# Kernel optimization log

Measured on AMD Instinct MI355X. Metric: run time of the kernel, lower is better.

Reference implementation:

```python
import jax, jax.numpy as jnp
import numpy as np
from jax import lax

B, N, D, FD = 1, 6, 128, 128
H = W = 64
FH, FW = 32, 96
QW1, QW2 = 8, 8
KW1, KW2 = 4, 12
HEADS, DH = 4, 32
IMG_H, IMG_W = 256, 768
BN_S = 0.9999950000374996  # eval-mode BatchNorm, default stats: 1/sqrt(1+1e-5)
LN_EPS = 1e-5


def _ln(x):
    mu = x.mean(-1, keepdims=True)
    var = ((x - mu) ** 2).mean(-1, keepdims=True)
    return (x - mu) * lax.rsqrt(var + LN_EPS)


def _gelu(x):
    return jax.nn.gelu(x, approximate=False)


def _win(t, w1, w2):
    # 'b n d (x w1) (y w2) -> b n x y w1 w2 d'
    b, n, d, h, w = t.shape
    t = t.reshape(b, n, d, h // w1, w1, w // w2, w2)
    return t.transpose(0, 1, 3, 5, 4, 6, 2)


def _gridwin(t, w1, w2):
    b, n, h, w, d = t.shape
    t = t.reshape(b, n, w1, h // w1, w2, w // w2, d)
    return t.transpose(0, 1, 3, 5, 2, 4, 6)


def _cross_attend(q, k, v, qw, qb, kw, kb, vw, vb, pw, pb, skip):
    b, n, X, Y, w1, w2, d = q.shape
    k1, k2 = k.shape[4], k.shape[5]
    L, Q, K = X * Y, n * w1 * w2, n * k1 * k2
    qf = q.transpose(0, 2, 3, 1, 4, 5, 6).reshape(b, L, Q, d)
    kf = k.transpose(0, 2, 3, 1, 4, 5, 6).reshape(b, L, K, d)
    vf = v.transpose(0, 2, 3, 1, 4, 5, 6).reshape(b, L, K, d)
    qh = (_ln(qf) @ qw.T + qb).reshape(b, L, Q, HEADS, DH)
    kh = (_ln(kf) @ kw.T + kb).reshape(b, L, K, HEADS, DH)
    vh = (_ln(vf) @ vw.T + vb).reshape(b, L, K, HEADS, DH)
    dot = jnp.einsum('blqmd,blkmd->bmlqk', qh, kh) * (DH ** -0.5)
    att = jax.nn.softmax(dot, axis=-1)
    a = jnp.einsum('bmlqk,blkmd->blqmd', att, vh).reshape(b, L, Q, HEADS * DH)
    z = (a @ pw.T + pb).reshape(b, X, Y, n, w1, w2, d).mean(3)
    return z + skip


def reference(index, x, feature, I_inv, E_inv, bev_grid, fl_w, fp_w, be_w, be_b, ie_w, ce_w,
              a1_qw, a1_qb, a1_kw, a1_kb, a1_vw, a1_vb, a1_pw, a1_pb,
              a2_qw, a2_qb, a2_kw, a2_kb, a2_vw, a2_vb, a2_pw, a2_pb,
              m1_w1, m1_b1, m1_w2, m1_b2, m2_w1, m2_b1, m2_w2, m2_b2,
              mb_ew, mb_dw, mb_s1w, mb_s1b, mb_s2w, mb_s2b, mb_pw,
              pm_w1, pm_b1, pm_w2, pm_b2, po_w, po_b):
    # image-plane rays -> camera-frame directions
    xs = jnp.linspace(0.0, 1.0, FW) * IMG_W
    ys = jnp.linspace(0.0, 1.0, FH) * IMG_H
    gx, gy = jnp.meshgrid(xs, ys)                       # [FH,FW]
    pixel = jnp.stack([gx, gy, jnp.ones_like(gx)], 0).reshape(3, FH * FW)
    cam = jnp.einsum('bnij,jp->bnip', I_inv, pixel)     # [B,N,3,P]
    cam = jnp.concatenate([cam, jnp.ones_like(cam[:, :, :1])], axis=2)
    dvec = jnp.einsum('bnij,bnjp->bnip', E_inv, cam).reshape(B, N, 4, FH, FW)
    d_embed = jnp.einsum('bnchw,dc->bndhw', dvec, ie_w)            # img_embed 1x1 conv
    c_embed = jnp.einsum('bnc,dc->bnd', E_inv[..., 3], ce_w)[:, :, :, None, None]
    img_emb = d_embed - c_embed
    img_emb = img_emb / (jnp.linalg.norm(img_emb, axis=2, keepdims=True) + 1e-7)

    # BEV positional embedding (bev_embedding_flag[index] True)
    w_embed = jnp.einsum('chw,dc->dhw', bev_grid[:2], be_w) + be_b[:, None, None]
    bev_emb = w_embed[None, None] - c_embed                        # [B,N,D,H,W]
    bev_emb = bev_emb / (jnp.linalg.norm(bev_emb, axis=2, keepdims=True) + 1e-7)
    query = bev_emb + x[:, None]

    # key/value (BatchNorm eval -> ReLU -> 1x1 conv)
    f = jax.nn.relu(feature * BN_S)
    key = img_emb + jnp.einsum('bnchw,dc->bndhw', f, fp_w)
    val = jnp.einsum('bnchw,dc->bndhw', f, fl_w)

    # local-to-local windowed cross attention
    skip1 = _win(x[:, None], QW1, QW2)[:, 0]
    out1 = _cross_attend(_win(query, QW1, QW2), _win(key, KW1, KW2), _win(val, KW1, KW2),
                         a1_qw, a1_qb, a1_kw, a1_kb, a1_vw, a1_vb, a1_pw, a1_pb, skip1)
    q_img = out1.transpose(0, 1, 3, 2, 4, 5).reshape(B, H, W, D)   # 'b x y w1 w2 d -> b (x w1)(y w2) d'
    q_img = q_img + (_gelu(_ln(q_img) @ m1_w1.T + m1_b1) @ m1_w2.T + m1_b2)

    # local-to-global (grid-shuffled windows)
    x_skip = q_img
    q2 = jnp.broadcast_to(q_img[:, None], (B, N, H, W, D))
    key_hwd = key.transpose(0, 1, 3, 4, 2)
    val_hwd = val.transpose(0, 1, 3, 4, 2)
    skip2 = _gridwin(x_skip[:, None], QW1, QW2)[:, 0]
    out2 = _cross_attend(_gridwin(q2, QW1, QW2), _gridwin(key_hwd, KW1, KW2), _gridwin(val_hwd, KW1, KW2),
                         a2_qw, a2_qb, a2_kw, a2_kb, a2_vw, a2_vb, a2_pw, a2_pb, skip2)
    q_img = out2.transpose(0, 3, 1, 4, 2, 5).reshape(B, H, W, D)
    q_img = q_img + (_gelu(_ln(q_img) @ m2_w1.T + m2_b1) @ m2_w2.T + m2_b2)

    z = _ln(q_img)                                   # postnorm
    zc = z.transpose(0, 3, 1, 2)                     # [B,D,H,W]
    # MBConv (expand -> depthwise -> SE -> project, eval-mode BN, residual)
    out = _gelu(jnp.einsum('bchw,dc->bdhw', zc, mb_ew) * BN_S)
    out = lax.conv_general_dilated(out, mb_dw, (1, 1), 'SAME',
                                   dimension_numbers=('NCHW', 'OIHW', 'NCHW'),
                                   feature_group_count=out.shape[1])
    out = _gelu(out * BN_S)
    se = out.mean((2, 3), keepdims=True)
    se = _gelu(jnp.einsum('bchw,dc->bdhw', se, mb_s1w) + mb_s1b[None, :, None, None])
    se = jax.nn.sigmoid(jnp.einsum('bchw,dc->bdhw', se, mb_s2w) + mb_s2b[None, :, None, None])
    out = jnp.einsum('bchw,dc->bdhw', out * se, mb_pw) * BN_S + zc
    z = out.transpose(0, 2, 3, 1)                    # [B,H,W,D]
    z = z + (_gelu(z @ pm_w1.T + pm_b1) @ pm_w2.T + pm_b2)   # ChannelFFN
    z = _gelu(z @ po_w.T + po_b)                     # proj_out
    return z.transpose(0, 3, 1, 2)                   # [B,D,H,W]


def setup_inputs():
    ks = iter(jax.random.split(jax.random.key(0), 80))

    def rn(*s):
        return jax.random.normal(next(ks), s, dtype=jnp.float32) * 0.02

    def zz(*s):
        return jnp.zeros(s, dtype=jnp.float32)

    inp = {
        'index': 0,
        'x': jax.random.normal(next(ks), (B, D, H, W), dtype=jnp.float32),
        'feature': jax.random.normal(next(ks), (B, N, FD, FH, FW), dtype=jnp.float32),
        'I_inv': jax.random.normal(next(ks), (B, N, 3, 3), dtype=jnp.float32),
        'E_inv': jax.random.normal(next(ks), (B, N, 4, 4), dtype=jnp.float32),
        'bev_grid': jax.random.uniform(next(ks), (3, H, W), dtype=jnp.float32),
        'fl_w': rn(D, FD), 'fp_w': rn(D, FD),
        'be_w': rn(D, 2), 'be_b': zz(D), 'ie_w': rn(D, 4), 'ce_w': rn(D, 4),
    }
    for p in ('a1', 'a2'):
        for nm in ('q', 'k', 'v'):
            inp[p + '_' + nm + 'w'] = rn(HEADS * DH, D)
            inp[p + '_' + nm + 'b'] = zz(HEADS * DH)
        inp[p + '_pw'] = rn(D, HEADS * DH)
        inp[p + '_pb'] = zz(D)
    for p in ('m1', 'm2'):
        inp[p + '_w1'] = rn(2 * D, D)
        inp[p + '_b1'] = zz(2 * D)
        inp[p + '_w2'] = rn(D, 2 * D)
        inp[p + '_b2'] = zz(D)
    inp.update(mb_ew=rn(4 * D, D), mb_dw=rn(4 * D, 1, 3, 3),
               mb_s1w=rn(32, 4 * D), mb_s1b=zz(32), mb_s2w=rn(4 * D, 32), mb_s2b=zz(4 * D),
               mb_pw=rn(D, 4 * D),
               pm_w1=rn(2 * D, D), pm_b1=zz(2 * D), pm_w2=rn(D, 2 * D), pm_b2=zz(D),
               po_w=rn(D, D), po_b=zz(D))
    return inp
```

## Files before the change

kernel.cpp:

```cpp
#include <hip/hip_runtime.h>
#include <math.h>

#define NV 6
#define FHH 32
#define FWW 96
#define PIMG (FHH*FWW)
#define HH 64
#define WWD 64
#define PBEV (HH*WWD)
#define HEADS 4
#define DHD 32
#define KROWS 288
#define BN_S 0.9999950000374996f
#define LN_EPS 1e-5f
#define ATT_SCALE 0.17677669529663687f

typedef __attribute__((ext_vector_type(8))) short short8;
typedef __attribute__((ext_vector_type(4))) float f32x4;
typedef __attribute__((ext_vector_type(8))) unsigned short u16x8;

__device__ __forceinline__ float gelu_f(float x) {
    return 0.5f * x * (1.0f + erff(x * 0.70710678118654752f));
}

__device__ __forceinline__ unsigned short f2bf(float f) {
    union { float f; unsigned int u; } c; c.f = f;
    unsigned int r = (c.u + 0x7fffu + ((c.u >> 16) & 1u)) >> 16;
    return (unsigned short)r;
}

__device__ __forceinline__ float bf2f(unsigned short u) {
    union { unsigned int u; float f; } c; c.u = ((unsigned int)u) << 16;
    return c.f;
}

#define OFF_FP    0
#define OFF_FL    16384
#define OFF_A1QW  32768
#define OFF_A1KW  49152
#define OFF_A2KW  65536
#define OFF_A1VW  81920
#define OFF_A2VW  98304
#define OFF_A1PW  114688
#define OFF_M1W1  131072
#define OFF_M1W2  163840
#define OFF_A2QW  196608
#define OFF_A2PW  212992
#define OFF_M2W1  229376
#define OFF_M2W2  262144
#define OFF_MBEW  294912
#define OFF_MBPW  360448
#define OFF_PMW1  425984
#define OFF_PMW2  458752
#define OFF_POW   491520
#define WTOTAL    507904

__global__ void k_cvtw(const float* p0, const float* p1, const float* p2,
                       const float* p3, const float* p4, const float* p5,
                       const float* p6, const float* p7, const float* p8,
                       const float* p9, const float* p10, const float* p11,
                       const float* p12, const float* p13, const float* p14,
                       const float* p15, const float* p16, const float* p17,
                       const float* p18, unsigned short* wb) {
    int idx = (blockIdx.x * 256 + threadIdx.x) * 8;
    if (idx >= WTOTAL) return;
    const float* s;
    if      (idx < OFF_FL)   s = p0  + idx;
    else if (idx < OFF_A1QW) s = p1  + (idx - OFF_FL);
    else if (idx < OFF_A1KW) s = p2  + (idx - OFF_A1QW);
    else if (idx < OFF_A2KW) s = p3  + (idx - OFF_A1KW);
    else if (idx < OFF_A1VW) s = p4  + (idx - OFF_A2KW);
    else if (idx < OFF_A2VW) s = p5  + (idx - OFF_A1VW);
    else if (idx < OFF_A1PW) s = p6  + (idx - OFF_A2VW);
    else if (idx < OFF_M1W1) s = p7  + (idx - OFF_A1PW);
    else if (idx < OFF_M1W2) s = p8  + (idx - OFF_M1W1);
    else if (idx < OFF_A2QW) s = p9  + (idx - OFF_M1W2);
    else if (idx < OFF_A2PW) s = p10 + (idx - OFF_A2QW);
    else if (idx < OFF_M2W1) s = p11 + (idx - OFF_A2PW);
    else if (idx < OFF_M2W2) s = p12 + (idx - OFF_M2W1);
    else if (idx < OFF_MBEW) s = p13 + (idx - OFF_M2W2);
    else if (idx < OFF_MBPW) s = p14 + (idx - OFF_MBEW);
    else if (idx < OFF_PMW1) s = p15 + (idx - OFF_MBPW);
    else if (idx < OFF_PMW2) s = p16 + (idx - OFF_PMW1);
    else if (idx < OFF_POW)  s = p17 + (idx - OFF_PMW2);
    else                     s = p18 + (idx - OFF_POW);
    float4 v0 = *(const float4*)&s[0];
    float4 v1 = *(const float4*)&s[4];
    u16x8 o = { f2bf(v0.x), f2bf(v0.y), f2bf(v0.z), f2bf(v0.w),
                f2bf(v1.x), f2bf(v1.y), f2bf(v1.z), f2bf(v1.w) };
    *(u16x8*)&wb[idx] = o;
}

__global__ void k_transx(const float* __restrict__ x, float* __restrict__ x_cl) {
    __shared__ float tile[32][33];
    int c0 = blockIdx.y * 32, p0 = blockIdx.x * 32;
    int tp = threadIdx.x & 31, tg = threadIdx.x >> 5;
    #pragma unroll
    for (int i = 0; i < 4; ++i)
        tile[tg + 8 * i][tp] = x[(size_t)(c0 + tg + 8 * i) * PBEV + p0 + tp];
    __syncthreads();
    #pragma unroll
    for (int i = 0; i < 4; ++i)
        x_cl[(size_t)(p0 + tg + 8 * i) * 128 + c0 + tp] = tile[tp][tg + 8 * i];
}

template<int BR, int KCH, int NOT, int AMODE, int LNF, int BIASF, int ACT, int SCL,
         int ADDM, int STM, int ASCL, int DUAL, int OUTBF, int QSCL, int WRLN,
         int EMB, int WBF>
__global__ __launch_bounds__(256)
void k_gemm_mfma(const float* __restrict__ A, const float* __restrict__ W,
                 const float* __restrict__ bias, const float* __restrict__ addb,
                 const float* __restrict__ ascale, const float* __restrict__ W2,
                 const float* __restrict__ bias2, void* __restrict__ out2v,
                 float* __restrict__ aux, void* __restrict__ outv) {
    constexpr int NI = KCH * 128;
    constexpr int RW = BR / 16;
    constexpr int CT = 8 / (4 / RW);
    __shared__ unsigned short Al[BR * 136];
    __shared__ unsigned short Wl[128 * 136];
    const int t = threadIdx.x;
    const int rb = blockIdx.x * BR;
    const int co = blockIdx.y * 128;
    const int lane = t & 63, wv = t >> 6;
    const int la = lane & 15, g = lane >> 4;
    const int roww = wv % RW, colg = wv / RW;

    if constexpr (KCH == 1) {
        if constexpr (AMODE == 1) {
            int n = rb / PIMG, p0 = rb % PIMG;
            int r = t & 63, kseg = t >> 6;
            #pragma unroll
            for (int j8 = 0; j8 < 4; ++j8) {
                u16x8 o;
                #pragma unroll
                for (int j = 0; j < 8; ++j) {
                    int k = kseg * 32 + j8 * 8 + j;
                    float v = A[((size_t)(n * 128 + k)) * PIMG + p0 + r];
                    o[j] = f2bf(fmaxf(v * BN_S, 0.0f));
                }
                *(u16x8*)&Al[r * 136 + kseg * 32 + j8 * 8] = o;
            }
        } else {
            constexpr int TPR = 256 / BR;
            constexpr int CPT = 128 / TPR;
            int r = t / TPR, seg = t % TPR;
            float v[CPT];
            if constexpr (AMODE == 3) {
                int grow = rb + r;
                int n = grow >> 12, p = grow & 4095;
                const float* E = ((const float*)out2v) + n * 16;
                const float* cew = (const float*)aux;
                float bp0 = addb[p], bp1 = addb[PBEV + p];
                float ss = 0.f;
                #pragma unroll
                for (int j = 0; j < CPT; ++j) {
                    int c = seg * CPT + j;
                    float cemb = E[3]  * cew[c*4+0] + E[7]  * cew[c*4+1]
                               + E[11] * cew[c*4+2] + E[15] * cew[c*4+3];
                    float emb = bp0 * W2[c*2] + bp1 * W2[c*2+1] + bias2[c] - cemb;
                    v[j] = emb; ss += emb * emb;
                }
                #pragma unroll
                for (int o = 1; o < TPR; o <<= 1) ss += __shfl_xor(ss, o, 64);
                float invn = 1.0f / (sqrtf(ss) + 1e-7f);
                const float* xr = ascale + (size_t)p * 128 + seg * CPT;
                #pragma unroll
                for (int j = 0; j < CPT; ++j) v[j] = v[j] * invn + xr[j];
            } else if constexpr (AMODE == 4) {
                const unsigned short* ab = ((const unsigned short*)A)
                    + (size_t)(rb + r) * 128 + seg * CPT;
                #pragma unroll
                for (int j8 = 0; j8 < CPT / 8; ++j8) {
                    u16x8 raw = *(const u16x8*)&ab[8 * j8];
                    #pragma unroll
                    for (int j = 0; j < 8; ++j) v[8 * j8 + j] = bf2f(raw[j]);
                }
            } else {
                const float* ar = A + (size_t)(rb + r) * 128 + seg * CPT;
                #pragma unroll
                for (int j4 = 0; j4 < CPT / 4; ++j4)
                    *(float4*)&v[4 * j4] = *(const float4*)&ar[4 * j4];
            }
            if constexpr (LNF) {
                float s = 0.f;
                #pragma unroll
                for (int j = 0; j < CPT; ++j) s += v[j];
                #pragma unroll
                for (int o = 1; o < TPR; o <<= 1) s += __shfl_xor(s, o, 64);
                float mu = s * (1.0f / 128.0f);
                float ss = 0.f;
                #pragma unroll
                for (int j = 0; j < CPT; ++j) { float d = v[j] - mu; ss += d * d; }
                #pragma unroll
                for (int o = 1; o < TPR; o <<= 1) ss += __shfl_xor(ss, o, 64);
                float rs = rsqrtf(ss * (1.0f / 128.0f) + LN_EPS);
                #pragma unroll
                for (int j = 0; j < CPT; ++j) v[j] = (v[j] - mu) * rs;
                if constexpr (WRLN) {
                    if (blockIdx.y == 0) {
                        #pragma unroll
                        for (int j4 = 0; j4 < CPT / 4; ++j4) {
                            float4 o4 = {v[4*j4], v[4*j4+1], v[4*j4+2], v[4*j4+3]};
                            *(float4*)&aux[(size_t)(rb + r) * 128 + seg * CPT + 4 * j4] = o4;
                        }
                    }
                }
            }
            #pragma unroll
            for (int j8 = 0; j8 < CPT / 8; ++j8) {
                u16x8 o;
                #pragma unroll
                for (int j = 0; j < 8; ++j) o[j] = f2bf(v[8 * j8 + j]);
                *(u16x8*)&Al[r * 136 + seg * CPT + 8 * j8] = o;
            }
        }
    }

    #pragma unroll 1
    for (int set = 0; set <= DUAL; ++set) {
        const float* Wc = set ? W2 : W;
        const float* bc = set ? bias2 : bias;
        void* ocv = set ? out2v : outv;
        f32x4 acc[CT];
        #pragma unroll
        for (int i = 0; i < CT; ++i) acc[i] = (f32x4){0.f, 0.f, 0.f, 0.f};

        #pragma unroll 1
        for (int kc = 0; kc < KCH; ++kc) {
            if (set || kc) __syncthreads();
            #pragma unroll
            for (int i = 0; i < 8; ++i) {
                int chunk = i * 256 + t;
                int c = chunk >> 4, k8 = chunk & 15;
                if constexpr (WBF) {
                    const unsigned short* wr = ((const unsigned short*)Wc)
                        + (size_t)(co + c) * NI + kc * 128 + k8 * 8;
                    *(u16x8*)&Wl[c * 136 + k8 * 8] = *(const u16x8*)wr;
                } else {
                    const float* wr = &Wc[(size_t)(co + c) * NI + kc * 128 + k8 * 8];
                    float4 v0 = *(const float4*)&wr[0];
                    float4 v1 = *(const float4*)&wr[4];
                    u16x8 o = { f2bf(v0.x), f2bf(v0.y), f2bf(v0.z), f2bf(v0.w),
                                f2bf(v1.x), f2bf(v1.y), f2bf(v1.z), f2bf(v1.w) };
                    *(u16x8*)&Wl[c * 136 + k8 * 8] = o;
                }
            }
            __syncthreads();
            short8 af[4];
            #pragma unroll
            for (int ks = 0; ks < 4; ++ks)
                af[ks] = *(short8*)&Al[(roww * 16 + la) * 136 + ks * 32 + g * 8];
            #pragma unroll
            for (int cti = 0; cti < CT; ++cti) {
                int ct = colg * CT + cti;
                #pragma unroll
                for (int ks = 0; ks < 4; ++ks) {
                    short8 bf = *(short8*)&Wl[(ct * 16 + la) * 136 + ks * 32 + g * 8];
                    acc[cti] = __builtin_amdgcn_mfma_f32_16x16x32_bf16(af[ks], bf, acc[cti], 0, 0, 0);
                }
            }
        }

        float embv[CT][4];
        float invr[4];
        if constexpr (EMB) {
            if (set == 0) {
                int n = rb / PIMG;
                const float* Ii = ascale + n * 9;
                const float* E  = addb + n * 16;
                float d0[4], d1[4], d2[4], d3[4];
                #pragma unroll
                for (int r = 0; r < 4; ++r) {
                    int row = rb + roww * 16 + g * 4 + r;
                    int p = row % PIMG;
                    int hh = p / FWW, wp = p % FWW;
                    float gx = (float)wp * (768.0f / 95.0f);
                    float gy = (float)hh * (256.0f / 31.0f);
                    float c0 = Ii[0]*gx + Ii[1]*gy + Ii[2];
                    float c1 = Ii[3]*gx + Ii[4]*gy + Ii[5];
                    float c2 = Ii[6]*gx + Ii[7]*gy + Ii[8];
                    d0[r] = E[0]*c0  + E[1]*c1  + E[2]*c2  + E[3];
                    d1[r] = E[4]*c0  + E[5]*c1  + E[6]*c2  + E[7];
                    d2[r] = E[8]*c0  + E[9]*c1  + E[10]*c2 + E[11];
                    d3[r] = E[12]*c0 + E[13]*c1 + E[14]*c2 + E[15];
                }
                float ssr[4] = {0.f, 0.f, 0.f, 0.f};
                #pragma unroll
                for (int cti = 0; cti < CT; ++cti) {
                    int col = co + (colg * CT + cti) * 16 + la;
                    const float* iw = bias + col * 4;
                    const float* cw = bias2 + col * 4;
                    float cemb = E[3]*cw[0] + E[7]*cw[1] + E[11]*cw[2] + E[15]*cw[3];
                    #pragma unroll
                    for (int r = 0; r < 4; ++r) {
                        float e = d0[r]*iw[0] + d1[r]*iw[1] + d2[r]*iw[2] + d3[r]*iw[3] - cemb;
                        embv[cti][r] = e;
                        ssr[r] += e * e;
                    }
                }
                #pragma unroll
                for (int r = 0; r < 4; ++r) {
                    float s = ssr[r];
                    s += __shfl_xor(s, 1); s += __shfl_xor(s, 2);
                    s += __shfl_xor(s, 4); s += __shfl_xor(s, 8);
                    invr[r] = 1.0f / (sqrtf(s) + 1e-7f);
                }
            }
        }

        #pragma unroll
        for (int cti = 0; cti < CT; ++cti) {
            int ct = colg * CT + cti;
            int col = co + ct * 16 + la;
            float bv = 0.f;
            if constexpr (BIASF) bv = bc[col];
            if constexpr (STM == 1) {
                int row0 = rb + roww * 16 + g * 4;
                float vv[4];
                #pragma unroll
                for (int r = 0; r < 4; ++r) {
                    float v = acc[cti][r] + bv;
                    if constexpr (SCL)  v *= BN_S;
                    if constexpr (ACT)  v = gelu_f(v);
                    if constexpr (QSCL) v *= ATT_SCALE;
                    vv[r] = v;
                }
                float4 o4 = {vv[0], vv[1], vv[2], vv[3]};
                *(float4*)&((float*)ocv)[(size_t)col * PBEV + row0] = o4;
            } else {
                #pragma unroll
                for (int r = 0; r < 4; ++r) {
                    int row = rb + roww * 16 + g * 4 + r;
                    float v = acc[cti][r] + bv;
                    if constexpr (SCL)  v *= BN_S;
                    if constexpr (ACT)  v = gelu_f(v);
                    if constexpr (QSCL) v *= ATT_SCALE;
                    if constexpr (EMB) { if (set == 0) v += embv[cti][r] * invr[r]; }
                    if constexpr (ADDM == 1) { if (set == 0) v += addb[(size_t)row * 128 + col]; }
                    if constexpr (ADDM == 2) { if (set == 0) v += addb[(size_t)col * PBEV + row]; }
                    if constexpr (OUTBF) ((unsigned short*)ocv)[(size_t)row * NOT + col] = f2bf(v);
                    else                 ((float*)ocv)[(size_t)row * NOT + col] = v;
                }
            }
        }
    }
}

struct KVJob {
    const unsigned short* A;
    const unsigned short* W1;
    const float* b1;
    const unsigned short* W2;
    const float* b2;
    unsigned short* o1;
    unsigned short* o2;
};

__global__ __launch_bounds__(256)
void k_kvheads(KVJob jk, KVJob jv) {
    const KVJob j = (blockIdx.x < 288) ? jk : jv;
    const int rb = (blockIdx.x % 288) * 64;
    __shared__ unsigned short Al[64 * 136];
    __shared__ unsigned short Wl[128 * 136];
    const int t = threadIdx.x;
    const int lane = t & 63, wv = t >> 6;
    const int la = lane & 15, g = lane >> 4;

    {
        int r = t >> 2, seg = t & 3;
        const unsigned short* ab = j.A + (size_t)(rb + r) * 128 + seg * 32;
        float v[32];
        #pragma unroll
        for (int j8 = 0; j8 < 4; ++j8) {
            u16x8 raw = *(const u16x8*)&ab[8 * j8];
            #pragma unroll
            for (int jj = 0; jj < 8; ++jj) v[8 * j8 + jj] = bf2f(raw[jj]);
        }
        float s = 0.f;
        #pragma unroll
        for (int jj = 0; jj < 32; ++jj) s += v[jj];
        s += __shfl_xor(s, 1); s += __shfl_xor(s, 2);
        float mu = s * (1.0f / 128.0f);
        float ss = 0.f;
        #pragma unroll
        for (int jj = 0; jj < 32; ++jj) { float d = v[jj] - mu; ss += d * d; }
        ss += __shfl_xor(ss, 1); ss += __shfl_xor(ss, 2);
        float rs = rsqrtf(ss * (1.0f / 128.0f) + LN_EPS);
        #pragma unroll
        for (int j8 = 0; j8 < 4; ++j8) {
            u16x8 o;
            #pragma unroll
            for (int jj = 0; jj < 8; ++jj) o[jj] = f2bf((v[8 * j8 + jj] - mu) * rs);
            *(u16x8*)&Al[r * 136 + seg * 32 + 8 * j8] = o;
        }
    }

    #pragma unroll 1
    for (int set = 0; set < 2; ++set) {
        const unsigned short* Wc = set ? j.W2 : j.W1;
        const float* bc = set ? j.b2 : j.b1;
        unsigned short* oc = set ? j.o2 : j.o1;
        if (set) __syncthreads();
        #pragma unroll
        for (int i = 0; i < 8; ++i) {
            int chunk = i * 256 + t;
            int c = chunk >> 4, k8 = chunk & 15;
            *(u16x8*)&Wl[c * 136 + k8 * 8] =
                *(const u16x8*)&Wc[(size_t)c * 128 + k8 * 8];
        }
        __syncthreads();
        short8 af[4];
        #pragma unroll
        for (int ks = 0; ks < 4; ++ks)
            af[ks] = *(short8*)&Al[(wv * 16 + la) * 136 + ks * 32 + g * 8];
        #pragma unroll
        for (int ct = 0; ct < 8; ++ct) {
            f32x4 acc = (f32x4){0.f, 0.f, 0.f, 0.f};
            #pragma unroll
            for (int ks = 0; ks < 4; ++ks) {
                short8 bf = *(short8*)&Wl[(ct * 16 + la) * 136 + ks * 32 + g * 8];
                acc = __builtin_amdgcn_mfma_f32_16x16x32_bf16(af[ks], bf, acc, 0, 0, 0);
            }
            int col = ct * 16 + la;
            float bv = bc[col];
            #pragma unroll
            for (int r = 0; r < 4; ++r) {
                int row = rb + wv * 16 + g * 4 + r;
                oc[(size_t)row * 128 + col] = f2bf(acc[r] + bv);
            }
        }
    }
}

template<int AM>
__global__ __launch_bounds__(256)
void k_projmlp(const float* __restrict__ Ain, const unsigned short* __restrict__ pwb,
               const float* __restrict__ pb, const float* __restrict__ resid,
               const unsigned short* __restrict__ w1b, const float* __restrict__ b1,
               const unsigned short* __restrict__ w2b, const float* __restrict__ b2,
               float* __restrict__ out) {
    __shared__ unsigned short Al[16 * 136];
    __shared__ unsigned short Wl[128 * 72];
    __shared__ unsigned short Gl[16 * 264];
    __shared__ float Xf[16 * 132];
    const int t = threadIdx.x;
    const int rb = blockIdx.x * 16;
    const int lane = t & 63, wv = t >> 6;
    const int la = lane & 15, g = lane >> 4;

    {
        int r = t >> 4, seg = t & 15;
        float v[8];
        if constexpr (AM == 2) {
            int hw = rb + r;
            int h = hw >> 6, w = hw & 63;
            int l = (h >> 3) * 8 + (w >> 3), ww = (h & 7) * 8 + (w & 7);
            const float* src = Ain + ((size_t)(l * 64 + ww)) * 6 * 128 + seg * 8;
            #pragma unroll
            for (int jj = 0; jj < 8; ++jj) v[jj] = 0.f;
            #pragma unroll
            for (int n = 0; n < 6; ++n) {
                float4 x0 = *(const float4*)&src[n * 128];
                float4 x1 = *(const float4*)&src[n * 128 + 4];
                v[0] += x0.x; v[1] += x0.y; v[2] += x0.z; v[3] += x0.w;
                v[4] += x1.x; v[5] += x1.y; v[6] += x1.z; v[7] += x1.w;
            }
            #pragma unroll
            for (int jj = 0; jj < 8; ++jj) v[jj] *= (1.0f / 6.0f);
        } else {
            const float* ar = Ain + (size_t)(rb + r) * 128 + seg * 8;
            *(float4*)&v[0] = *(const float4*)&ar[0];
            *(float4*)&v[4] = *(const float4*)&ar[4];
        }
        u16x8 o;
        #pragma unroll
        for (int jj = 0; jj < 8; ++jj) o[jj] = f2bf(v[jj]);
        *(u16x8*)&Al[r * 136 + seg * 8] = o;
    }
    __syncthreads();

    f32x4 acc2[2];
    acc2[0] = (f32x4){0.f, 0.f, 0.f, 0.f};
    acc2[1] = (f32x4){0.f, 0.f, 0.f, 0.f};
    #pragma unroll 1
    for (int kc = 0; kc < 2; ++kc) {
        if (kc) __syncthreads();
        {
            int c = t >> 1, s2 = t & 1;
            const unsigned short* wr = pwb + (size_t)c * 128 + kc * 64 + s2 * 32;
            #pragma unroll
            for (int j8 = 0; j8 < 4; ++j8)
                *(u16x8*)&Wl[c * 72 + s2 * 32 + 8 * j8] = *(const u16x8*)&wr[8 * j8];
        }
        __syncthreads();
        #pragma unroll
        for (int half = 0; half < 2; ++half) {
            short8 pf = *(short8*)&Al[la * 136 + kc * 64 + half * 32 + g * 8];
            #pragma unroll
            for (int ct = 0; ct < 2; ++ct) {
                short8 bf = *(short8*)&Wl[((wv * 2 + ct) * 16 + la) * 72 + half * 32 + g * 8];
                acc2[ct] = __builtin_amdgcn_mfma_f32_16x16x32_bf16(pf, bf, acc2[ct], 0, 0, 0);
            }
        }
    }
    __syncthreads();
    #pragma unroll
    for (int ct = 0; ct < 2; ++ct) {
        int col = (wv * 2 + ct) * 16 + la;
        float bv = pb[col];
        #pragma unroll
        for (int r = 0; r < 4; ++r) {
            int row = g * 4 + r;
            Xf[row * 132 + col] = acc2[ct][r] + bv
                                + resid[(size_t)(rb + row) * 128 + col];
        }
    }
    __syncthreads();

    {
        int r = t >> 4, seg = t & 15;
        float v[8];
        #pragma unroll
        for (int jj = 0; jj < 8; ++jj) v[jj] = Xf[r * 132 + seg * 8 + jj];
        float s = 0.f;
        #pragma unroll
        for (int jj = 0; jj < 8; ++jj) s += v[jj];
        s += __shfl_xor(s, 1); s += __shfl_xor(s, 2);
        s += __shfl_xor(s, 4); s += __shfl_xor(s, 8);
        float mu = s * (1.0f / 128.0f);
        float ss = 0.f;
        #pragma unroll
        for (int jj = 0; jj < 8; ++jj) { float d = v[jj] - mu; ss += d * d; }
        ss += __shfl_xor(ss, 1); ss += __shfl_xor(ss, 2);
        ss += __shfl_xor(ss, 4); ss += __shfl_xor(ss, 8);
        float rs = rsqrtf(ss * (1.0f / 128.0f) + LN_EPS);
        u16x8 o;
        #pragma unroll
        for (int jj = 0; jj < 8; ++jj) o[jj] = f2bf((v[jj] - mu) * rs);
        *(u16x8*)&Al[r * 136 + seg * 8] = o;
    }
    __syncthreads();

    short8 af[4];
    #pragma unroll
    for (int ks = 0; ks < 4; ++ks)
        af[ks] = *(short8*)&Al[la * 136 + ks * 32 + g * 8];

    #pragma unroll 1
    for (int cc = 0; cc < 4; ++cc) {
        {
            int c = t >> 2, s2 = t & 3;
            const unsigned short* wr = w1b + (size_t)(cc * 64 + c) * 128 + s2 * 32;
            #pragma unroll
            for (int j8 = 0; j8 < 4; ++j8)
                *(u16x8*)&Wl[c * 136 + s2 * 32 + 8 * j8] = *(const u16x8*)&wr[8 * j8];
        }
        __syncthreads();
        f32x4 acc = (f32x4){0.f, 0.f, 0.f, 0.f};
        #pragma unroll
        for (int ks = 0; ks < 4; ++ks) {
            short8 bf = *(short8*)&Wl[(wv * 16 + la) * 136 + ks * 32 + g * 8];
            acc = __builtin_amdgcn_mfma_f32_16x16x32_bf16(af[ks], bf, acc, 0, 0, 0);
        }
        int col = cc * 64 + wv * 16 + la;
        float bv = b1[col];
        #pragma unroll
        for (int r = 0; r < 4; ++r)
            Gl[(g * 4 + r) * 264 + col] = f2bf(gelu_f(acc[r] + bv));
        __syncthreads();
    }

    acc2[0] = (f32x4){0.f, 0.f, 0.f, 0.f};
    acc2[1] = (f32x4){0.f, 0.f, 0.f, 0.f};
    #pragma unroll 1
    for (int kc = 0; kc < 4; ++kc) {
        {
            int c = t >> 1, s2 = t & 1;
            const unsigned short* wr = w2b + (size_t)c * 256 + kc * 64 + s2 * 32;
            #pragma unroll
            for (int j8 = 0; j8 < 4; ++j8)
                *(u16x8*)&Wl[c * 72 + s2 * 32 + 8 * j8] = *(const u16x8*)&wr[8 * j8];
        }
        __syncthreads();
        #pragma unroll
        for (int half = 0; half < 2; ++half) {
            short8 pf = *(short8*)&Gl[la * 264 + kc * 64 + half * 32 + g * 8];
            #pragma unroll
            for (int ct = 0; ct < 2; ++ct) {
                short8 bf = *(short8*)&Wl[((wv * 2 + ct) * 16 + la) * 72 + half * 32 + g * 8];
                acc2[ct] = __builtin_amdgcn_mfma_f32_16x16x32_bf16(pf, bf, acc2[ct], 0, 0, 0);
            }
        }
        __syncthreads();
    }
    #pragma unroll
    for (int ct = 0; ct < 2; ++ct) {
        int col = (wv * 2 + ct) * 16 + la;
        float bv = b2[col];
        #pragma unroll
        for (int r = 0; r < 4; ++r) {
            int row = g * 4 + r;
            out[(size_t)(rb + row) * 128 + col] = acc2[ct][r] + bv + Xf[row * 132 + col];
        }
    }
}

__global__ __launch_bounds__(256)
void k_mbprojmlp(const float* __restrict__ dwo, const unsigned short* __restrict__ mbpwb,
                 const float* __restrict__ se, const float* __restrict__ zln,
                 const unsigned short* __restrict__ w1b, const float* __restrict__ b1,
                 const unsigned short* __restrict__ w2b, const float* __restrict__ b2,
                 const unsigned short* __restrict__ pob, const float* __restrict__ pb,
                 float* __restrict__ out) {
    __shared__ unsigned short Al[16 * 136];
    __shared__ unsigned short Wl[128 * 72];
    __shared__ unsigned short Gl[16 * 264];
    __shared__ float Xf[16 * 132];
    const int t = threadIdx.x;
    const int rb = blockIdx.x * 16;
    const int lane = t & 63, wv = t >> 6;
    const int la = lane & 15, g = lane >> 4;

    f32x4 acc2[2];
    acc2[0] = (f32x4){0.f, 0.f, 0.f, 0.f};
    acc2[1] = (f32x4){0.f, 0.f, 0.f, 0.f};
    #pragma unroll 1
    for (int kc = 0; kc < 8; ++kc) {
        if (kc) __syncthreads();
        {
            int r = t >> 4, seg = t & 15;
            const float* ar = dwo + (size_t)(rb + r) * 512 + kc * 64 + seg * 4;
            float4 v = *(const float4*)ar;
            const float* sp = se + kc * 64 + seg * 4;
            v.x *= sp[0]; v.y *= sp[1]; v.z *= sp[2]; v.w *= sp[3];
            unsigned short* dst = &Al[r * 136 + seg * 4];
            dst[0] = f2bf(v.x); dst[1] = f2bf(v.y);
            dst[2] = f2bf(v.z); dst[3] = f2bf(v.w);
        }
        {
            int c = t >> 1, s2 = t & 1;
            const unsigned short* wr = mbpwb + (size_t)c * 512 + kc * 64 + s2 * 32;
            #pragma unroll
            for (int j8 = 0; j8 < 4; ++j8)
                *(u16x8*)&Wl[c * 72 + s2 * 32 + 8 * j8] = *(const u16x8*)&wr[8 * j8];
        }
        __syncthreads();
        #pragma unroll
        for (int half = 0; half < 2; ++half) {
            short8 pf = *(short8*)&Al[la * 136 + half * 32 + g * 8];
            #pragma unroll
            for (int ct = 0; ct < 2; ++ct) {
                short8 bf = *(short8*)&Wl[((wv * 2 + ct) * 16 + la) * 72 + half * 32 + g * 8];
                acc2[ct] = __builtin_amdgcn_mfma_f32_16x16x32_bf16(pf, bf, acc2[ct], 0, 0, 0);
            }
        }
    }
    __syncthreads();
    #pragma unroll
    for (int ct = 0; ct < 2; ++ct) {
        int col = (wv * 2 + ct) * 16 + la;
        #pragma unroll
        for (int r = 0; r < 4; ++r) {
            int row = g * 4 + r;
            Xf[row * 132 + col] = acc2[ct][r] * BN_S
                                + zln[(size_t)(rb + row) * 128 + col];
        }
    }
    __syncthreads();

    {
        int r = t >> 4, seg = t & 15;
        u16x8 o;
        #pragma unroll
        for (int jj = 0; jj < 8; ++jj) o[jj] = f2bf(Xf[r * 132 + seg * 8 + jj]);
        *(u16x8*)&Al[r * 136 + seg * 8] = o;
    }
    __syncthreads();

    short8 af[4];
    #pragma unroll
    for (int ks = 0; ks < 4; ++ks)
        af[ks] = *(short8*)&Al[la * 136 + ks * 32 + g * 8];

    #pragma unroll 1
    for (int cc = 0; cc < 4; ++cc) {
        {
            int c = t >> 2, s2 = t & 3;
            const unsigned short* wr = w1b + (size_t)(cc * 64 + c) * 128 + s2 * 32;
            #pragma unroll
            for (int j8 = 0; j8 < 4; ++j8)
                *(u16x8*)&Wl[c * 136 + s2 * 32 + 8 * j8] = *(const u16x8*)&wr[8 * j8];
        }
        __syncthreads();
        f32x4 acc = (f32x4){0.f, 0.f, 0.f, 0.f};
        #pragma unroll
        for (int ks = 0; ks < 4; ++ks) {
            short8 bf = *(short8*)&Wl[(wv * 16 + la) * 136 + ks * 32 + g * 8];
            acc = __builtin_amdgcn_mfma_f32_16x16x32_bf16(af[ks], bf, acc, 0, 0, 0);
        }
        int col = cc * 64 + wv * 16 + la;
        float bv = b1[col];
        #pragma unroll
        for (int r = 0; r < 4; ++r)
            Gl[(g * 4 + r) * 264 + col] = f2bf(gelu_f(acc[r] + bv));
        __syncthreads();
    }

    acc2[0] = (f32x4){0.f, 0.f, 0.f, 0.f};
    acc2[1] = (f32x4){0.f, 0.f, 0.f, 0.f};
    #pragma unroll 1
    for (int kc = 0; kc < 4; ++kc) {
        {
            int c = t >> 1, s2 = t & 1;
            const unsigned short* wr = w2b + (size_t)c * 256 + kc * 64 + s2 * 32;
            #pragma unroll
            for (int j8 = 0; j8 < 4; ++j8)
                *(u16x8*)&Wl[c * 72 + s2 * 32 + 8 * j8] = *(const u16x8*)&wr[8 * j8];
        }
        __syncthreads();
        #pragma unroll
        for (int half = 0; half < 2; ++half) {
            short8 pf = *(short8*)&Gl[la * 264 + kc * 64 + half * 32 + g * 8];
            #pragma unroll
            for (int ct = 0; ct < 2; ++ct) {
                short8 bf = *(short8*)&Wl[((wv * 2 + ct) * 16 + la) * 72 + half * 32 + g * 8];
                acc2[ct] = __builtin_amdgcn_mfma_f32_16x16x32_bf16(pf, bf, acc2[ct], 0, 0, 0);
            }
        }
        __syncthreads();
    }
    #pragma unroll
    for (int ct = 0; ct < 2; ++ct) {
        int col = (wv * 2 + ct) * 16 + la;
        float bv = b2[col];
        #pragma unroll
        for (int r = 0; r < 4; ++r) {
            int row = g * 4 + r;
            float y = acc2[ct][r] + bv + Xf[row * 132 + col];
            Al[row * 136 + col] = f2bf(y);
        }
    }
    __syncthreads();

    f32x4 acc3[2];
    acc3[0] = (f32x4){0.f, 0.f, 0.f, 0.f};
    acc3[1] = (f32x4){0.f, 0.f, 0.f, 0.f};
    #pragma unroll 1
    for (int kc = 0; kc < 2; ++kc) {
        if (kc) __syncthreads();
        {
            int c = t >> 1, s2 = t & 1;
            const unsigned short* wr = pob + (size_t)c * 128 + kc * 64 + s2 * 32;
            #pragma unroll
            for (int j8 = 0; j8 < 4; ++j8)
                *(u16x8*)&Wl[c * 72 + s2 * 32 + 8 * j8] = *(const u16x8*)&wr[8 * j8];
        }
        __syncthreads();
        #pragma unroll
        for (int half = 0; half < 2; ++half) {
            short8 pf = *(short8*)&Al[la * 136 + kc * 64 + half * 32 + g * 8];
            #pragma unroll
            for (int ct = 0; ct < 2; ++ct) {
                short8 bf = *(short8*)&Wl[((wv * 2 + ct) * 16 + la) * 72 + half * 32 + g * 8];
                acc3[ct] = __builtin_amdgcn_mfma_f32_16x16x32_bf16(pf, bf, acc3[ct], 0, 0, 0);
            }
        }
    }
    #pragma unroll
    for (int ct = 0; ct < 2; ++ct) {
        int col = (wv * 2 + ct) * 16 + la;
        float bv = pb[col];
        float4 o4;
        o4.x = gelu_f(acc3[ct][0] + bv);
        o4.y = gelu_f(acc3[ct][1] + bv);
        o4.z = gelu_f(acc3[ct][2] + bv);
        o4.w = gelu_f(acc3[ct][3] + bv);
        *(float4*)&out[(size_t)col * PBEV + rb + g * 4] = o4;
    }
}

template<int MODE>
__global__ __launch_bounds__(MODE == 1 ? 512 : 256)
void k_attn_mfma(const unsigned short* __restrict__ qh, const unsigned short* __restrict__ kh,
                 const unsigned short* __restrict__ vh, float* __restrict__ aout) {
    constexpr int WAVES = (MODE == 1) ? 8 : 4;
    constexpr int QTPW  = (MODE == 1) ? 3 : 1;
    constexpr int T = WAVES * 64;
    const int l = blockIdx.x, m = blockIdx.y;
    const int xw = l >> 3, yw = l & 7;
    const int t = threadIdx.x;
    const int lane = t & 63, wv = t >> 6;
    const int la = lane & 15, g = lane >> 4;

    __shared__ unsigned short Kl[KROWS * 40];
    __shared__ unsigned short Vt[32 * 312];

    for (int i = t; i < KROWS * 4; i += T) {
        int row = i >> 2, seg = i & 3;
        int n = row / 48, kk = row % 48;
        int k1 = kk / 12, k2 = kk % 12;
        int h, w;
        if (MODE == 1) { h = xw * 4 + k1;  w = yw * 12 + k2; }
        else           { h = k1 * 8 + xw;  w = k2 * 8 + yw;  }
        size_t src = ((size_t)(n * PIMG + h * FWW + w)) * 128 + m * DHD + seg * 8;
        short8 kv = *(const short8*)&kh[src];
        *(short8*)&Kl[row * 40 + seg * 8] = kv;
        short8 vv = *(const short8*)&vh[src];
        #pragma unroll
        for (int j = 0; j < 8; ++j)
            Vt[(seg * 8 + j) * 312 + row] = (unsigned short)vv[j];
    }

    short8 qf[QTPW];
    #pragma unroll
    for (int qt = 0; qt < QTPW; ++qt) {
        int q = (wv * QTPW + qt) * 16 + la;
        int row;
        if (MODE == 1) {
            int n = q >> 6, ww = q & 63;
            row = n * PBEV + (xw * 8 + (ww >> 3)) * 64 + yw * 8 + (ww & 7);
        } else {
            row = ((q >> 3) * 8 + xw) * 64 + (q & 7) * 8 + yw;
        }
        qf[qt] = *(const short8*)&qh[(size_t)row * 128 + m * DHD + g * 8];
    }
    __syncthreads();

    f32x4 acc[QTPW][2];
    float srow[QTPW];
    #pragma unroll
    for (int qt = 0; qt < QTPW; ++qt) {
        acc[qt][0] = (f32x4){0.f, 0.f, 0.f, 0.f};
        acc[qt][1] = (f32x4){0.f, 0.f, 0.f, 0.f};
        srow[qt] = 0.f;
    }
    const int a0 = la + 32 * (g & 1);
    const int a1 = a0 + 16;
    const bool selA = (g < 2);

    #pragma unroll 1
    for (int c = 0; c < 9; ++c) {
        const int kk0 = c * 32;
        short8 kf0 = *(short8*)&Kl[(kk0 + la) * 40 + g * 8];
        short8 kf1 = *(short8*)&Kl[(kk0 + 16 + la) * 40 + g * 8];
        short8 vf0 = *(short8*)&Vt[la * 312 + kk0 + g * 8];
        short8 vf1 = *(short8*)&Vt[(16 + la) * 312 + kk0 + g * 8];
        #pragma unroll
        for (int qt = 0; qt < QTPW; ++qt) {
            f32x4 sA = __builtin_amdgcn_mfma_f32_16x16x32_bf16(kf0, qf[qt], (f32x4){0.f,0.f,0.f,0.f}, 0, 0, 0);
            f32x4 sB = __builtin_amdgcn_mfma_f32_16x16x32_bf16(kf1, qf[qt], (f32x4){0.f,0.f,0.f,0.f}, 0, 0, 0);
            float pA[4], pB[4];
            #pragma unroll
            for (int r = 0; r < 4; ++r) { pA[r] = __expf(sA[r]); pB[r] = __expf(sB[r]); }
            srow[qt] += ((pA[0] + pA[1]) + (pA[2] + pA[3]))
                      + ((pB[0] + pB[1]) + (pB[2] + pB[3]));
            unsigned int loA = (unsigned int)f2bf(pA[0]) | ((unsigned int)f2bf(pA[1]) << 16);
            unsigned int hiA = (unsigned int)f2bf(pA[2]) | ((unsigned int)f2bf(pA[3]) << 16);
            unsigned int loB = (unsigned int)f2bf(pB[0]) | ((unsigned int)f2bf(pB[1]) << 16);
            unsigned int hiB = (unsigned int)f2bf(pB[2]) | ((unsigned int)f2bf(pB[3]) << 16);
            int w0A = __shfl((int)loA, a0); int w0B = __shfl((int)loB, a0);
            int w1A = __shfl((int)hiA, a0); int w1B = __shfl((int)hiB, a0);
            int w2A = __shfl((int)loA, a1); int w2B = __shfl((int)loB, a1);
            int w3A = __shfl((int)hiA, a1); int w3B = __shfl((int)hiB, a1);
            union { int u[4]; short8 s; } pu;
            pu.u[0] = selA ? w0A : w0B;
            pu.u[1] = selA ? w1A : w1B;
            pu.u[2] = selA ? w2A : w2B;
            pu.u[3] = selA ? w3A : w3B;
            acc[qt][0] = __builtin_amdgcn_mfma_f32_16x16x32_bf16(pu.s, vf0, acc[qt][0], 0, 0, 0);
            acc[qt][1] = __builtin_amdgcn_mfma_f32_16x16x32_bf16(pu.s, vf1, acc[qt][1], 0, 0, 0);
        }
    }

    #pragma unroll
    for (int qt = 0; qt < QTPW; ++qt) {
        float s = srow[qt];
        s += __shfl_xor(s, 16);
        s += __shfl_xor(s, 32);
        #pragma unroll
        for (int r = 0; r < 4; ++r) {
            float sq = __shfl(s, g * 4 + r);
            float inv = 1.0f / sq;
            int q = (wv * QTPW + qt) * 16 + g * 4 + r;
            size_t orow;
            if (MODE == 1) {
                int n = q >> 6, ww = q & 63;
                orow = (size_t)(l * 64 + ww) * 6 + n;
            } else {
                orow = (size_t)(((q >> 3) * 8 + xw) * 64 + (q & 7) * 8 + yw);
            }
            float* ap = aout + orow * 128 + m * DHD;
            ap[la]      = acc[qt][0][r] * inv;
            ap[16 + la] = acc[qt][1][r] * inv;
        }
    }
}

__global__ void k_dwconv(const float* __restrict__ ex, const float* __restrict__ dwgt,
                         float* __restrict__ dwout, float* __restrict__ separt) {
    const int TILE = 16;
    int ch = threadIdx.x;
    int hw0 = blockIdx.x * TILE;
    float wreg[9];
    #pragma unroll
    for (int i = 0; i < 9; ++i) wreg[i] = dwgt[ch * 9 + i];
    float sacc = 0.f;
    for (int ti = 0; ti < TILE; ++ti) {
        int hw = hw0 + ti;
        int h = hw >> 6, w = hw & 63;
        float s = 0.f;
        #pragma unroll
        for (int dy = -1; dy <= 1; ++dy) {
            int h2 = h + dy;
            if (h2 < 0 || h2 >= 64) continue;
            #pragma unroll
            for (int dx = -1; dx <= 1; ++dx) {
                int w2 = w + dx;
                if (w2 < 0 || w2 >= 64) continue;
                s += ex[((size_t)(h2 * 64 + w2)) * 512 + ch] * wreg[(dy + 1) * 3 + (dx + 1)];
            }
        }
        float o = gelu_f(s * BN_S);
        dwout[(size_t)hw * 512 + ch] = o;
        sacc += o;
    }
    separt[(size_t)blockIdx.x * 512 + ch] = sacc;
}

__global__ void k_sered(const float* __restrict__ separt, float* __restrict__ separt2) {
    int t = threadIdx.x, bb = blockIdx.x;
    float s = 0.f;
    #pragma unroll
    for (int i = 0; i < 16; ++i)
        s += separt[(size_t)(bb * 16 + i) * 512 + t];
    separt2[(size_t)bb * 512 + t] = s;
}

__global__ void k_se(const float* __restrict__ separt2,
                     const float* __restrict__ s1w, const float* __restrict__ s1b,
                     const float* __restrict__ s2w, const float* __restrict__ s2b,
                     float* __restrict__ se) {
    __shared__ float mean[512];
    __shared__ float s1[32];
    int t = threadIdx.x;
    float s = 0.f;
    #pragma unroll
    for (int b = 0; b < 16; ++b) s += separt2[b * 512 + t];
    mean[t] = s * (1.0f / 4096.0f);
    __syncthreads();
    int u = t >> 4, seg = t & 15;
    float acc = 0.f;
    #pragma unroll
    for (int j = 0; j < 32; ++j) {
        int c = seg + 16 * j;
        acc += mean[c] * s1w[u * 512 + c];
    }
    acc += __shfl_xor(acc, 1); acc += __shfl_xor(acc, 2);
    acc += __shfl_xor(acc, 4); acc += __shfl_xor(acc, 8);
    if (seg == 0) s1[u] = gelu_f(acc + s1b[u]);
    __syncthreads();
    float a2 = s2b[t];
    #pragma unroll
    for (int j = 0; j < 32; ++j) a2 += s1[j] * s2w[t * 32 + j];
    se[t] = 1.0f / (1.0f + __expf(-a2));
}

extern "C" void kernel_launch(void* const* d_in, const int* in_sizes, int n_in,
                              void* d_out, int out_size, void* d_ws, size_t ws_size,
                              hipStream_t stream) {
    (void)in_sizes; (void)n_in; (void)out_size; (void)ws_size;
    const float* x      = (const float*)d_in[1];
    const float* feat   = (const float*)d_in[2];
    const float* I_inv  = (const float*)d_in[3];
    const float* E_inv  = (const float*)d_in[4];
    const float* bev    = (const float*)d_in[5];
    const float* fl_w   = (const float*)d_in[6];
    const float* fp_w   = (const float*)d_in[7];
    const float* be_w   = (const float*)d_in[8];
    const float* be_b   = (const float*)d_in[9];
    const float* ie_w   = (const float*)d_in[10];
    const float* ce_w   = (const float*)d_in[11];
    const float* a1_qw  = (const float*)d_in[12];
    const float* a1_qb  = (const float*)d_in[13];
    const float* a1_kw  = (const float*)d_in[14];
    const float* a1_kb  = (const float*)d_in[15];
    const float* a1_vw  = (const float*)d_in[16];
    const float* a1_vb  = (const float*)d_in[17];
    const float* a1_pw  = (const float*)d_in[18];
    const float* a1_pb  = (const float*)d_in[19];
    const float* a2_qw  = (const float*)d_in[20];
    const float* a2_qb  = (const float*)d_in[21];
    const float* a2_kw  = (const float*)d_in[22];
    const float* a2_kb  = (const float*)d_in[23];
    const float* a2_vw  = (const float*)d_in[24];
    const float* a2_vb  = (const float*)d_in[25];
    const float* a2_pw  = (const float*)d_in[26];
    const float* a2_pb  = (const float*)d_in[27];
    const float* m1_w1  = (const float*)d_in[28];
    const float* m1_b1  = (const float*)d_in[29];
    const float* m1_w2  = (const float*)d_in[30];
    const float* m1_b2  = (const float*)d_in[31];
    const float* m2_w1  = (const float*)d_in[32];
    const float* m2_b1  = (const float*)d_in[33];
    const float* m2_w2  = (const float*)d_in[34];
    const float* m2_b2  = (const float*)d_in[35];
    const float* mb_ew  = (const float*)d_in[36];
    const float* mb_dw  = (const float*)d_in[37];
    const float* mb_s1w = (const float*)d_in[38];
    const float* mb_s1b = (const float*)d_in[39];
    const float* mb_s2w = (const float*)d_in[40];
    const float* mb_s2b = (const float*)d_in[41];
    const float* mb_pw  = (const float*)d_in[42];
    const float* pm_w1  = (const float*)d_in[43];
    const float* pm_b1  = (const float*)d_in[44];
    const float* pm_w2  = (const float*)d_in[45];
    const float* pm_b2  = (const float*)d_in[46];
    const float* po_w   = (const float*)d_in[47];
    const float* po_b   = (const float*)d_in[48];

    float* ws = (float*)d_ws;
    float* x_cl   = ws + 0;
    unsigned short* key_b = (unsigned short*)(ws + 524288);
    unsigned short* val_b = (unsigned short*)(ws + 1703936);
    unsigned short* qh1b  = (unsigned short*)(ws + 2883584);
    unsigned short* kh1b  = (unsigned short*)(ws + 4456448);
    unsigned short* vh1b  = (unsigned short*)(ws + 5636096);
    unsigned short* kh2b  = (unsigned short*)(ws + 6815744);
    unsigned short* vh2b  = (unsigned short*)(ws + 7995392);
    float* abuf   = ws + 9175040;
    float* qimg   = ws + 12320768;
    float* qimg2  = ws + 12845056;
    float* zln    = ws + 13369344;
    float* abuf2  = ws + 13893632;
    float* expandb = ws + 14942208;
    float* dwout   = ws + 17039360;
    float* separt  = ws + 19136512;
    float* separt2 = ws + 19267584;
    float* sebuf   = ws + 19275776;
    unsigned short* wb = (unsigned short*)(ws + 19276288);
    unsigned short* qh2b = qh1b;

    k_cvtw<<<248, 256, 0, stream>>>(fp_w, fl_w, a1_qw, a1_kw, a2_kw, a1_vw, a2_vw,
                                    a1_pw, m1_w1, m1_w2, a2_qw, a2_pw, m2_w1, m2_w2,
                                    mb_ew, mb_pw, pm_w1, pm_w2, po_w, wb);
    k_transx<<<dim3(128, 4), 256, 0, stream>>>(x, x_cl);

    k_gemm_mfma<64,1,128, 1,0,0,0,0, 0,0,0,1, 1,0,0,1,1><<<288, 256, 0, stream>>>(
        feat, (const float*)(wb + OFF_FP), ie_w, E_inv, I_inv,
        (const float*)(wb + OFF_FL), ce_w, val_b, nullptr, key_b);

    k_gemm_mfma<64,1,128, 3,1,1,0,0, 0,0,0,0, 1,1,0,0,1><<<384, 256, 0, stream>>>(
        nullptr, (const float*)(wb + OFF_A1QW), a1_qb, bev, x_cl, be_w, be_b,
        (void*)E_inv, (float*)ce_w, qh1b);
    {
        KVJob jk = { key_b, wb + OFF_A1KW, a1_kb, wb + OFF_A2KW, a2_kb, kh1b, kh2b };
        KVJob jv = { val_b, wb + OFF_A1VW, a1_vb, wb + OFF_A2VW, a2_vb, vh1b, vh2b };
        k_kvheads<<<576, 256, 0, stream>>>(jk, jv);
    }
    k_attn_mfma<1><<<dim3(64, HEADS), 512, 0, stream>>>(qh1b, kh1b, vh1b, abuf);
    k_projmlp<2><<<256, 256, 0, stream>>>(abuf, wb + OFF_A1PW, a1_pb, x_cl,
                                          wb + OFF_M1W1, m1_b1, wb + OFF_M1W2, m1_b2, qimg);

    k_gemm_mfma<16,1,128, 0,1,1,0,0, 0,0,0,0, 1,1,0,0,1><<<256, 256, 0, stream>>>(
        qimg, (const float*)(wb + OFF_A2QW), a2_qb, nullptr, nullptr, nullptr,
        nullptr, nullptr, nullptr, qh2b);
    k_attn_mfma<2><<<dim3(64, HEADS), 256, 0, stream>>>(qh2b, kh2b, vh2b, abuf2);
    k_projmlp<0><<<256, 256, 0, stream>>>(abuf2, wb + OFF_A2PW, a2_pb, qimg,
                                          wb + OFF_M2W1, m2_b1, wb + OFF_M2W2, m2_b2, qimg2);

    k_gemm_mfma<16,1,512, 0,1,0,1,1, 0,0,0,0, 0,0,1,0,1><<<dim3(256, 4), 256, 0, stream>>>(
        qimg2, (const float*)(wb + OFF_MBEW), nullptr, nullptr, nullptr, nullptr,
        nullptr, nullptr, zln, expandb);
    k_dwconv<<<256, 512, 0, stream>>>(expandb, mb_dw, dwout, separt);
    k_sered<<<16, 512, 0, stream>>>(separt, separt2);
    k_se<<<1, 512, 0, stream>>>(separt2, mb_s1w, mb_s1b, mb_s2w, mb_s2b, sebuf);
    k_mbprojmlp<<<256, 256, 0, stream>>>(dwout, wb + OFF_MBPW, sebuf, zln,
                                         wb + OFF_PMW1, pm_b1, wb + OFF_PMW2, pm_b2,
                                         wb + OFF_POW, po_b, (float*)d_out);
}
```

Before: 155.2 us.

## Fuse key/value feature and head projections, merge prep kernels, average views in attention

Weight conversion and the BEV transpose are merged into one launch. The feature-to-key/value GEMMs, camera embedding, LayerNorm and all four per-head K/V projections now run in a single kernel that keeps intermediates in shared memory, so the key_b/val_b round trip through global memory goes away. The first attention reduces the per-view mean in shared memory with atomics and writes an averaged buffer, which lets the projection-MLP skip that averaging. The SE partial-sum kernel is folded into the SE kernel. Together these cut launches and memory traffic, at the cost of serial per-block work and shared-memory atomics.

```diff
diff --git a/kernel.cpp b/kernel.cpp
--- a/kernel.cpp
+++ b/kernel.cpp
@@ -27,11 +27,6 @@
     union { float f; unsigned int u; } c; c.f = f;
     unsigned int r = (c.u + 0x7fffu + ((c.u >> 16) & 1u)) >> 16;
     return (unsigned short)r;
-}
-
-__device__ __forceinline__ float bf2f(unsigned short u) {
-    union { unsigned int u; float f; } c; c.u = ((unsigned int)u) << 16;
-    return c.f;
 }
 
 #define OFF_FP    0
@@ -55,65 +50,232 @@
 #define OFF_POW   491520
 #define WTOTAL    507904
 
-__global__ void k_cvtw(const float* p0, const float* p1, const float* p2,
+__global__ void k_prep(const float* p0, const float* p1, const float* p2,
                        const float* p3, const float* p4, const float* p5,
                        const float* p6, const float* p7, const float* p8,
                        const float* p9, const float* p10, const float* p11,
                        const float* p12, const float* p13, const float* p14,
                        const float* p15, const float* p16, const float* p17,
-                       const float* p18, unsigned short* wb) {
-    int idx = (blockIdx.x * 256 + threadIdx.x) * 8;
-    if (idx >= WTOTAL) return;
-    const float* s;
-    if      (idx < OFF_FL)   s = p0  + idx;
-    else if (idx < OFF_A1QW) s = p1  + (idx - OFF_FL);
-    else if (idx < OFF_A1KW) s = p2  + (idx - OFF_A1QW);
-    else if (idx < OFF_A2KW) s = p3  + (idx - OFF_A1KW);
-    else if (idx < OFF_A1VW) s = p4  + (idx - OFF_A2KW);
-    else if (idx < OFF_A2VW) s = p5  + (idx - OFF_A1VW);
-    else if (idx < OFF_A1PW) s = p6  + (idx - OFF_A2VW);
-    else if (idx < OFF_M1W1) s = p7  + (idx - OFF_A1PW);
-    else if (idx < OFF_M1W2) s = p8  + (idx - OFF_M1W1);
-    else if (idx < OFF_A2QW) s = p9  + (idx - OFF_M1W2);
-    else if (idx < OFF_A2PW) s = p10 + (idx - OFF_A2QW);
-    else if (idx < OFF_M2W1) s = p11 + (idx - OFF_A2PW);
-    else if (idx < OFF_M2W2) s = p12 + (idx - OFF_M2W1);
-    else if (idx < OFF_MBEW) s = p13 + (idx - OFF_M2W2);
-    else if (idx < OFF_MBPW) s = p14 + (idx - OFF_MBEW);
-    else if (idx < OFF_PMW1) s = p15 + (idx - OFF_MBPW);
-    else if (idx < OFF_PMW2) s = p16 + (idx - OFF_PMW1);
-    else if (idx < OFF_POW)  s = p17 + (idx - OFF_PMW2);
-    else                     s = p18 + (idx - OFF_POW);
-    float4 v0 = *(const float4*)&s[0];
-    float4 v1 = *(const float4*)&s[4];
-    u16x8 o = { f2bf(v0.x), f2bf(v0.y), f2bf(v0.z), f2bf(v0.w),
-                f2bf(v1.x), f2bf(v1.y), f2bf(v1.z), f2bf(v1.w) };
-    *(u16x8*)&wb[idx] = o;
+                       const float* p18, unsigned short* wb,
+                       const float* __restrict__ x, float* __restrict__ x_cl) {
+    __shared__ float tile[32][33];
+    if (blockIdx.x < 248) {
+        int idx = (blockIdx.x * 256 + threadIdx.x) * 8;
+        if (idx >= WTOTAL) return;
+        const float* s;
+        if      (idx < OFF_FL)   s = p0  + idx;
+        else if (idx < OFF_A1QW) s = p1  + (idx - OFF_FL);
+        else if (idx < OFF_A1KW) s = p2  + (idx - OFF_A1QW);
+        else if (idx < OFF_A2KW) s = p3  + (idx - OFF_A1KW);
+        else if (idx < OFF_A1VW) s = p4  + (idx - OFF_A2KW);
+        else if (idx < OFF_A2VW) s = p5  + (idx - OFF_A1VW);
+        else if (idx < OFF_A1PW) s = p6  + (idx - OFF_A2VW);
+        else if (idx < OFF_M1W1) s = p7  + (idx - OFF_A1PW);
+        else if (idx < OFF_M1W2) s = p8  + (idx - OFF_M1W1);
+        else if (idx < OFF_A2QW) s = p9  + (idx - OFF_M1W2);
+        else if (idx < OFF_A2PW) s = p10 + (idx - OFF_A2QW);
+        else if (idx < OFF_M2W1) s = p11 + (idx - OFF_A2PW);
+        else if (idx < OFF_M2W2) s = p12 + (idx - OFF_M2W1);
+        else if (idx < OFF_MBEW) s = p13 + (idx - OFF_M2W2);
+        else if (idx < OFF_MBPW) s = p14 + (idx - OFF_MBEW);
+        else if (idx < OFF_PMW1) s = p15 + (idx - OFF_MBPW);
+        else if (idx < OFF_PMW2) s = p16 + (idx - OFF_PMW1);
+        else if (idx < OFF_POW)  s = p17 + (idx - OFF_PMW2);
+        else                     s = p18 + (idx - OFF_POW);
+        float4 v0 = *(const float4*)&s[0];
+        float4 v1 = *(const float4*)&s[4];
+        u16x8 o = { f2bf(v0.x), f2bf(v0.y), f2bf(v0.z), f2bf(v0.w),
+                    f2bf(v1.x), f2bf(v1.y), f2bf(v1.z), f2bf(v1.w) };
+        *(u16x8*)&wb[idx] = o;
+    } else {
+        int bb = blockIdx.x - 248;
+        int p0_ = (bb & 127) * 32, c0 = (bb >> 7) * 32;
+        int tp = threadIdx.x & 31, tg = threadIdx.x >> 5;
+        #pragma unroll
+        for (int i = 0; i < 4; ++i)
+            tile[tg + 8 * i][tp] = x[(size_t)(c0 + tg + 8 * i) * PBEV + p0_ + tp];
+        __syncthreads();
+        #pragma unroll
+        for (int i = 0; i < 4; ++i)
+            x_cl[(size_t)(p0_ + tg + 8 * i) * 128 + c0 + tp] = tile[tp][tg + 8 * i];
+    }
 }
 
-__global__ void k_transx(const float* __restrict__ x, float* __restrict__ x_cl) {
-    __shared__ float tile[32][33];
-    int c0 = blockIdx.y * 32, p0 = blockIdx.x * 32;
-    int tp = threadIdx.x & 31, tg = threadIdx.x >> 5;
-    #pragma unroll
-    for (int i = 0; i < 4; ++i)
-        tile[tg + 8 * i][tp] = x[(size_t)(c0 + tg + 8 * i) * PBEV + p0 + tp];
-    __syncthreads();
-    #pragma unroll
-    for (int i = 0; i < 4; ++i)
-        x_cl[(size_t)(p0 + tg + 8 * i) * 128 + c0 + tp] = tile[tp][tg + 8 * i];
+__global__ __launch_bounds__(256)
+void k_keyval(const float* __restrict__ feat, const unsigned short* __restrict__ wb,
+              const float* __restrict__ ie_w, const float* __restrict__ ce_w,
+              const float* __restrict__ I_inv, const float* __restrict__ E_inv,
+              const float* __restrict__ a1_kb, const float* __restrict__ a2_kb,
+              const float* __restrict__ a1_vb, const float* __restrict__ a2_vb,
+              unsigned short* __restrict__ kh1b, unsigned short* __restrict__ kh2b,
+              unsigned short* __restrict__ vh1b, unsigned short* __restrict__ vh2b) {
+    __shared__ unsigned short Al[64 * 136];
+    __shared__ unsigned short Bl[64 * 136];
+    __shared__ unsigned short Wl[128 * 136];
+    const int t = threadIdx.x;
+    const int rb = blockIdx.x * 64;
+    const int n = rb / PIMG;
+    const int lane = t & 63, wv = t >> 6;
+    const int la = lane & 15, g = lane >> 4;
+
+    {
+        int p0 = rb % PIMG;
+        int r = t & 63, kseg = t >> 6;
+        #pragma unroll
+        for (int j8 = 0; j8 < 4; ++j8) {
+            u16x8 o;
+            #pragma unroll
+            for (int j = 0; j < 8; ++j) {
+                int k = kseg * 32 + j8 * 8 + j;
+                float v = feat[((size_t)(n * 128 + k)) * PIMG + p0 + r];
+                o[j] = f2bf(fmaxf(v * BN_S, 0.0f));
+            }
+            *(u16x8*)&Al[r * 136 + kseg * 32 + j8 * 8] = o;
+        }
+    }
+
+    float d0[4], d1[4], d2[4], d3[4];
+    {
+        const float* Ii = I_inv + n * 9;
+        const float* E  = E_inv + n * 16;
+        #pragma unroll
+        for (int r = 0; r < 4; ++r) {
+            int row = rb + wv * 16 + g * 4 + r;
+            int p = row % PIMG;
+            int hh = p / FWW, wp = p % FWW;
+            float gx = (float)wp * (768.0f / 95.0f);
+            float gy = (float)hh * (256.0f / 31.0f);
+            float c0 = Ii[0]*gx + Ii[1]*gy + Ii[2];
+            float c1 = Ii[3]*gx + Ii[4]*gy + Ii[5];
+            float c2 = Ii[6]*gx + Ii[7]*gy + Ii[8];
+            d0[r] = E[0]*c0  + E[1]*c1  + E[2]*c2  + E[3];
+            d1[r] = E[4]*c0  + E[5]*c1  + E[6]*c2  + E[7];
+            d2[r] = E[8]*c0  + E[9]*c1  + E[10]*c2 + E[11];
+            d3[r] = E[12]*c0 + E[13]*c1 + E[14]*c2 + E[15];
+        }
+    }
+
+    #pragma unroll 1
+    for (int kv = 0; kv < 2; ++kv) {
+        __syncthreads();
+        {
+            const unsigned short* Wf = wb + (kv ? OFF_FL : OFF_FP);
+            #pragma unroll
+            for (int i = 0; i < 8; ++i) {
+                int chunk = i * 256 + t;
+                int c = chunk >> 4, k8 = chunk & 15;
+                *(u16x8*)&Wl[c * 136 + k8 * 8] = *(const u16x8*)&Wf[(size_t)c * 128 + k8 * 8];
+            }
+        }
+        __syncthreads();
+        short8 af[4];
+        #pragma unroll
+        for (int ks = 0; ks < 4; ++ks)
+            af[ks] = *(short8*)&Al[(wv * 16 + la) * 136 + ks * 32 + g * 8];
+        float vacc[8][4];
+        #pragma unroll
+        for (int ct = 0; ct < 8; ++ct) {
+            f32x4 a = (f32x4){0.f, 0.f, 0.f, 0.f};
+            #pragma unroll
+            for (int ks = 0; ks < 4; ++ks) {
+                short8 bf = *(short8*)&Wl[(ct * 16 + la) * 136 + ks * 32 + g * 8];
+                a = __builtin_amdgcn_mfma_f32_16x16x32_bf16(af[ks], bf, a, 0, 0, 0);
+            }
+            #pragma unroll
+            for (int r = 0; r < 4; ++r) vacc[ct][r] = a[r];
+        }
+        if (kv == 0) {
+            const float* E = E_inv + n * 16;
+            float embv[8][4];
+            float ssr[4] = {0.f, 0.f, 0.f, 0.f};
+            #pragma unroll
+            for (int ct = 0; ct < 8; ++ct) {
+                int col = ct * 16 + la;
+                const float* iw = ie_w + col * 4;
+                const float* cw = ce_w + col * 4;
+                float cemb = E[3]*cw[0] + E[7]*cw[1] + E[11]*cw[2] + E[15]*cw[3];
+                #pragma unroll
+                for (int r = 0; r < 4; ++r) {
+                    float e = d0[r]*iw[0] + d1[r]*iw[1] + d2[r]*iw[2] + d3[r]*iw[3] - cemb;
+                    embv[ct][r] = e;
+                    ssr[r] += e * e;
+                }
+            }
+            #pragma unroll
+            for (int r = 0; r < 4; ++r) {
+                float s = ssr[r];
+                s += __shfl_xor(s, 1); s += __shfl_xor(s, 2);
+                s += __shfl_xor(s, 4); s += __shfl_xor(s, 8);
+                float inv = 1.0f / (sqrtf(s) + 1e-7f);
+                #pragma unroll
+                for (int ct = 0; ct < 8; ++ct) vacc[ct][r] += embv[ct][r] * inv;
+            }
+        }
+        #pragma unroll
+        for (int r = 0; r < 4; ++r) {
+            float s = 0.f;
+            #pragma unroll
+            for (int ct = 0; ct < 8; ++ct) s += vacc[ct][r];
+            s += __shfl_xor(s, 1); s += __shfl_xor(s, 2);
+            s += __shfl_xor(s, 4); s += __shfl_xor(s, 8);
+            float mu = s * (1.0f / 128.0f);
+            float ss = 0.f;
+            #pragma unroll
+            for (int ct = 0; ct < 8; ++ct) { float d = vacc[ct][r] - mu; ss += d * d; }
+            ss += __shfl_xor(ss, 1); ss += __shfl_xor(ss, 2);
+            ss += __shfl_xor(ss, 4); ss += __shfl_xor(ss, 8);
+            float rs = rsqrtf(ss * (1.0f / 128.0f) + LN_EPS);
+            int brow = wv * 16 + g * 4 + r;
+            #pragma unroll
+            for (int ct = 0; ct < 8; ++ct)
+                Bl[brow * 136 + ct * 16 + la] = f2bf((vacc[ct][r] - mu) * rs);
+        }
+
+        #pragma unroll 1
+        for (int hs = 0; hs < 2; ++hs) {
+            __syncthreads();
+            const unsigned short* Wh = wb + (kv == 0 ? (hs ? OFF_A2KW : OFF_A1KW)
+                                                     : (hs ? OFF_A2VW : OFF_A1VW));
+            const float* hb = kv == 0 ? (hs ? a2_kb : a1_kb) : (hs ? a2_vb : a1_vb);
+            unsigned short* oc = kv == 0 ? (hs ? kh2b : kh1b) : (hs ? vh2b : vh1b);
+            #pragma unroll
+            for (int i = 0; i < 8; ++i) {
+                int chunk = i * 256 + t;
+                int c = chunk >> 4, k8 = chunk & 15;
+                *(u16x8*)&Wl[c * 136 + k8 * 8] = *(const u16x8*)&Wh[(size_t)c * 128 + k8 * 8];
+            }
+            __syncthreads();
+            short8 af2[4];
+            #pragma unroll
+            for (int ks = 0; ks < 4; ++ks)
+                af2[ks] = *(short8*)&Bl[(wv * 16 + la) * 136 + ks * 32 + g * 8];
+            #pragma unroll
+            for (int ct = 0; ct < 8; ++ct) {
+                f32x4 a = (f32x4){0.f, 0.f, 0.f, 0.f};
+                #pragma unroll
+                for (int ks = 0; ks < 4; ++ks) {
+                    short8 bf = *(short8*)&Wl[(ct * 16 + la) * 136 + ks * 32 + g * 8];
+                    a = __builtin_amdgcn_mfma_f32_16x16x32_bf16(af2[ks], bf, a, 0, 0, 0);
+                }
+                int col = ct * 16 + la;
+                float bv = hb[col];
+                #pragma unroll
+                for (int r = 0; r < 4; ++r)
+                    oc[(size_t)(rb + wv * 16 + g * 4 + r) * 128 + col] = f2bf(a[r] + bv);
+            }
+        }
+    }
 }
 
-template<int BR, int KCH, int NOT, int AMODE, int LNF, int BIASF, int ACT, int SCL,
-         int ADDM, int STM, int ASCL, int DUAL, int OUTBF, int QSCL, int WRLN,
-         int EMB, int WBF>
+template<int BR, int NOT, int AMODE, int LNF, int BIASF, int ACT, int SCL,
+         int OUTBF, int QSCL, int WRLN>
 __global__ __launch_bounds__(256)
-void k_gemm_mfma(const float* __restrict__ A, const float* __restrict__ W,
-                 const float* __restrict__ bias, const float* __restrict__ addb,
-                 const float* __restrict__ ascale, const float* __restrict__ W2,
-                 const float* __restrict__ bias2, void* __restrict__ out2v,
-                 float* __restrict__ aux, void* __restrict__ outv) {
-    constexpr int NI = KCH * 128;
+void k_gemm_mfma(const float* __restrict__ A, const unsigned short* __restrict__ Wb,
+                 const float* __restrict__ bias, const float* __restrict__ bev,
+                 const float* __restrict__ x_cl, const float* __restrict__ be_w,
+                 const float* __restrict__ be_b, const float* __restrict__ E_inv,
+                 const float* __restrict__ ce_w, float* __restrict__ aux,
+                 void* __restrict__ outv) {
     constexpr int RW = BR / 16;
     constexpr int CT = 8 / (4 / RW);
     __shared__ unsigned short Al[BR * 136];
@@ -125,314 +287,108 @@
     const int la = lane & 15, g = lane >> 4;
     const int roww = wv % RW, colg = wv / RW;
 
-    if constexpr (KCH == 1) {
-        if constexpr (AMODE == 1) {
-            int n = rb / PIMG, p0 = rb % PIMG;
-            int r = t & 63, kseg = t >> 6;
-            #pragma unroll
-            for (int j8 = 0; j8 < 4; ++j8) {
-                u16x8 o;
-                #pragma unroll
-                for (int j = 0; j < 8; ++j) {
-                    int k = kseg * 32 + j8 * 8 + j;
-                    float v = A[((size_t)(n * 128 + k)) * PIMG + p0 + r];
-                    o[j] = f2bf(fmaxf(v * BN_S, 0.0f));
-                }
-                *(u16x8*)&Al[r * 136 + kseg * 32 + j8 * 8] = o;
-            }
+    {
+        constexpr int TPR = 256 / BR;
+        constexpr int CPT = 128 / TPR;
+        int r = t / TPR, seg = t % TPR;
+        float v[CPT];
+        if constexpr (AMODE == 3) {
+            int grow = rb + r;
+            int n = grow >> 12, p = grow & 4095;
+            const float* E = E_inv + n * 16;
+            float bp0 = bev[p], bp1 = bev[PBEV + p];
+            float ss = 0.f;
+            #pragma unroll
+            for (int j = 0; j < CPT; ++j) {
+                int c = seg * CPT + j;
+                float cemb = E[3]  * ce_w[c*4+0] + E[7]  * ce_w[c*4+1]
+                           + E[11] * ce_w[c*4+2] + E[15] * ce_w[c*4+3];
+                float emb = bp0 * be_w[c*2] + bp1 * be_w[c*2+1] + be_b[c] - cemb;
+                v[j] = emb; ss += emb * emb;
+            }
+            #pragma unroll
+            for (int o = 1; o < TPR; o <<= 1) ss += __shfl_xor(ss, o, 64);
+            float invn = 1.0f / (sqrtf(ss) + 1e-7f);
+            const float* xr = x_cl + (size_t)p * 128 + seg * CPT;
+            #pragma unroll
+            for (int j = 0; j < CPT; ++j) v[j] = v[j] * invn + xr[j];
         } else {
-            constexpr int TPR = 256 / BR;
-            constexpr int CPT = 128 / TPR;
-            int r = t / TPR, seg = t % TPR;
-            float v[CPT];
-            if constexpr (AMODE == 3) {
-                int grow = rb + r;
-                int n = grow >> 12, p = grow & 4095;
-                const float* E = ((const float*)out2v) + n * 16;
-                const float* cew = (const float*)aux;
-                float bp0 = addb[p], bp1 = addb[PBEV + p];
-                float ss = 0.f;
-                #pragma unroll
-                for (int j = 0; j < CPT; ++j) {
-                    int c = seg * CPT + j;
-                    float cemb = E[3]  * cew[c*4+0] + E[7]  * cew[c*4+1]
-                               + E[11] * cew[c*4+2] + E[15] * cew[c*4+3];
-                    float emb = bp0 * W2[c*2] + bp1 * W2[c*2+1] + bias2[c] - cemb;
-                    v[j] = emb; ss += emb * emb;
-                }
-                #pragma unroll
-                for (int o = 1; o < TPR; o <<= 1) ss += __shfl_xor(ss, o, 64);
-                float invn = 1.0f / (sqrtf(ss) + 1e-7f);
-                const float* xr = ascale + (size_t)p * 128 + seg * CPT;
-                #pragma unroll
-                for (int j = 0; j < CPT; ++j) v[j] = v[j] * invn + xr[j];
-            } else if constexpr (AMODE == 4) {
-                const unsigned short* ab = ((const unsigned short*)A)
-                    + (size_t)(rb + r) * 128 + seg * CPT;
-                #pragma unroll
-                for (int j8 = 0; j8 < CPT / 8; ++j8) {
-                    u16x8 raw = *(const u16x8*)&ab[8 * j8];
+            const float* ar = A + (size_t)(rb + r) * 128 + seg * CPT;
+            #pragma unroll
+            for (int j4 = 0; j4 < CPT / 4; ++j4)
+                *(float4*)&v[4 * j4] = *(const float4*)&ar[4 * j4];
+        }
+        if constexpr (LNF) {
+            float s = 0.f;
+            #pragma unroll
+            for (int j = 0; j < CPT; ++j) s += v[j];
+            #pragma unroll
+            for (int o = 1; o < TPR; o <<= 1) s += __shfl_xor(s, o, 64);
+            float mu = s * (1.0f / 128.0f);
+            float ss = 0.f;
+            #pragma unroll
+            for (int j = 0; j < CPT; ++j) { float d = v[j] - mu; ss += d * d; }
+            #pragma unroll
+            for (int o = 1; o < TPR; o <<= 1) ss += __shfl_xor(ss, o, 64);
+            float rs = rsqrtf(ss * (1.0f / 128.0f) + LN_EPS);
+            #pragma unroll
+            for (int j = 0; j < CPT; ++j) v[j] = (v[j] - mu) * rs;
+            if constexpr (WRLN) {
+                if (blockIdx.y == 0) {
                     #pragma unroll
-                    for (int j = 0; j < 8; ++j) v[8 * j8 + j] = bf2f(raw[j]);
-                }
-            } else {
-                const float* ar = A + (size_t)(rb + r) * 128 + seg * CPT;
-                #pragma unroll
-                for (int j4 = 0; j4 < CPT / 4; ++j4)
-                    *(float4*)&v[4 * j4] = *(const float4*)&ar[4 * j4];
-            }
-            if constexpr (LNF) {
-                float s = 0.f;
-                #pragma unroll
-                for (int j = 0; j < CPT; ++j) s += v[j];
-                #pragma unroll
-                for (int o = 1; o < TPR; o <<= 1) s += __shfl_xor(s, o, 64);
-                float mu = s * (1.0f / 128.0f);
-                float ss = 0.f;
-                #pragma unroll
-                for (int j = 0; j < CPT; ++j) { float d = v[j] - mu; ss += d * d; }
-                #pragma unroll
-                for (int o = 1; o < TPR; o <<= 1) ss += __shfl_xor(ss, o, 64);
-                float rs = rsqrtf(ss * (1.0f / 128.0f) + LN_EPS);
-                #pragma unroll
-                for (int j = 0; j < CPT; ++j) v[j] = (v[j] - mu) * rs;
-                if constexpr (WRLN) {
-                    if (blockIdx.y == 0) {
-                        #pragma unroll
-                        for (int j4 = 0; j4 < CPT / 4; ++j4) {
-                            float4 o4 = {v[4*j4], v[4*j4+1], v[4*j4+2], v[4*j4+3]};
-                            *(float4*)&aux[(size_t)(rb + r) * 128 + seg * CPT + 4 * j4] = o4;
-                        }
+                    for (int j4 = 0; j4 < CPT / 4; ++j4) {
+                        float4 o4 = {v[4*j4], v[4*j4+1], v[4*j4+2], v[4*j4+3]};
+                        *(float4*)&aux[(size_t)(rb + r) * 128 + seg * CPT + 4 * j4] = o4;
                     }
                 }
             }
-            #pragma unroll
-            for (int j8 = 0; j8 < CPT / 8; ++j8) {
-                u16x8 o;
-                #pragma unroll
-                for (int j = 0; j < 8; ++j) o[j] = f2bf(v[8 * j8 + j]);
-                *(u16x8*)&Al[r * 136 + seg * CPT + 8 * j8] = o;
-            }
-        }
-    }
-
-    #pragma unroll 1
-    for (int set = 0; set <= DUAL; ++set) {
-        const float* Wc = set ? W2 : W;
-        const float* bc = set ? bias2 : bias;
-        void* ocv = set ? out2v : outv;
-        f32x4 acc[CT];
-        #pragma unroll
-        for (int i = 0; i < CT; ++i) acc[i] = (f32x4){0.f, 0.f, 0.f, 0.f};
-
-        #pragma unroll 1
-        for (int kc = 0; kc < KCH; ++kc) {
-            if (set || kc) __syncthreads();
-            #pragma unroll
-            for (int i = 0; i < 8; ++i) {
-                int chunk = i * 256 + t;
-                int c = chunk >> 4, k8 = chunk & 15;
-                if constexpr (WBF) {
-                    const unsigned short* wr = ((const unsigned short*)Wc)
-                        + (size_t)(co + c) * NI + kc * 128 + k8 * 8;
-                    *(u16x8*)&Wl[c * 136 + k8 * 8] = *(const u16x8*)wr;
-                } else {
-                    const float* wr = &Wc[(size_t)(co + c) * NI + kc * 128 + k8 * 8];
-                    float4 v0 = *(const float4*)&wr[0];
-                    float4 v1 = *(const float4*)&wr[4];
-                    u16x8 o = { f2bf(v0.x), f2bf(v0.y), f2bf(v0.z), f2bf(v0.w),
-                                f2bf(v1.x), f2bf(v1.y), f2bf(v1.z), f2bf(v1.w) };
-                    *(u16x8*)&Wl[c * 136 + k8 * 8] = o;
-                }
-            }
-            __syncthreads();
-            short8 af[4];
-            #pragma unroll
-            for (int ks = 0; ks < 4; ++ks)
-                af[ks] = *(short8*)&Al[(roww * 16 + la) * 136 + ks * 32 + g * 8];
-            #pragma unroll
-            for (int cti = 0; cti < CT; ++cti) {
-                int ct = colg * CT + cti;
-                #pragma unroll
-                for (int ks = 0; ks < 4; ++ks) {
-                    short8 bf = *(short8*)&Wl[(ct * 16 + la) * 136 + ks * 32 + g * 8];
-                    acc[cti] = __builtin_amdgcn_mfma_f32_16x16x32_bf16(af[ks], bf, acc[cti], 0, 0, 0);
-                }
-            }
-        }
-
-        float embv[CT][4];
-        float invr[4];
-        if constexpr (EMB) {
-            if (set == 0) {
-                int n = rb / PIMG;
-                const float* Ii = ascale + n * 9;
-                const float* E  = addb + n * 16;
-                float d0[4], d1[4], d2[4], d3[4];
-                #pragma unroll
-                for (int r = 0; r < 4; ++r) {
-                    int row = rb + roww * 16 + g * 4 + r;
-                    int p = row % PIMG;
-                    int hh = p / FWW, wp = p % FWW;
-                    float gx = (float)wp * (768.0f / 95.0f);
-                    float gy = (float)hh * (256.0f / 31.0f);
-                    float c0 = Ii[0]*gx + Ii[1]*gy + Ii[2];
-                    float c1 = Ii[3]*gx + Ii[4]*gy + Ii[5];
-                    float c2 = Ii[6]*gx + Ii[7]*gy + Ii[8];
-                    d0[r] = E[0]*c0  + E[1]*c1  + E[2]*c2  + E[3];
-                    d1[r] = E[4]*c0  + E[5]*c1  + E[6]*c2  + E[7];
-                    d2[r] = E[8]*c0  + E[9]*c1  + E[10]*c2 + E[11];
-                    d3[r] = E[12]*c0 + E[13]*c1 + E[14]*c2 + E[15];
-                }
-                float ssr[4] = {0.f, 0.f, 0.f, 0.f};
-                #pragma unroll
-                for (int cti = 0; cti < CT; ++cti) {
-                    int col = co + (colg * CT + cti) * 16 + la;
-                    const float* iw = bias + col * 4;
-                    const float* cw = bias2 + col * 4;
-                    float cemb = E[3]*cw[0] + E[7]*cw[1] + E[11]*cw[2] + E[15]*cw[3];
-                    #pragma unroll
-                    for (int r = 0; r < 4; ++r) {
-                        float e = d0[r]*iw[0] + d1[r]*iw[1] + d2[r]*iw[2] + d3[r]*iw[3] - cemb;
-                        embv[cti][r] = e;
-                        ssr[r] += e * e;
-                    }
-                }
-                #pragma unroll
-                for (int r = 0; r < 4; ++r) {
-                    float s = ssr[r];
-                    s += __shfl_xor(s, 1); s += __shfl_xor(s, 2);
-                    s += __shfl_xor(s, 4); s += __shfl_xor(s, 8);
-                    invr[r] = 1.0f / (sqrtf(s) + 1e-7f);
-                }
-            }
-        }
-
-        #pragma unroll
-        for (int cti = 0; cti < CT; ++cti) {
-            int ct = colg * CT + cti;
-            int col = co + ct * 16 + la;
-            float bv = 0.f;
-            if constexpr (BIASF) bv = bc[col];
-            if constexpr (STM == 1) {
-                int row0 = rb + roww * 16 + g * 4;
-                float vv[4];
-                #pragma unroll
-                for (int r = 0; r < 4; ++r) {
-                    float v = acc[cti][r] + bv;
-                    if constexpr (SCL)  v *= BN_S;
-                    if constexpr (ACT)  v = gelu_f(v);
-                    if constexpr (QSCL) v *= ATT_SCALE;
-                    vv[r] = v;
-                }
-                float4 o4 = {vv[0], vv[1], vv[2], vv[3]};
-                *(float4*)&((float*)ocv)[(size_t)col * PBEV + row0] = o4;
-            } else {
-                #pragma unroll
-                for (int r = 0; r < 4; ++r) {
-                    int row = rb + roww * 16 + g * 4 + r;
-                    float v = acc[cti][r] + bv;
-                    if constexpr (SCL)  v *= BN_S;
-                    if constexpr (ACT)  v = gelu_f(v);
-                    if constexpr (QSCL) v *= ATT_SCALE;
-                    if constexpr (EMB) { if (set == 0) v += embv[cti][r] * invr[r]; }
-                    if constexpr (ADDM == 1) { if (set == 0) v += addb[(size_t)row * 128 + col]; }
-                    if constexpr (ADDM == 2) { if (set == 0) v += addb[(size_t)col * PBEV + row]; }
-                    if constexpr (OUTBF) ((unsigned short*)ocv)[(size_t)row * NOT + col] = f2bf(v);
-                    else                 ((float*)ocv)[(size_t)row * NOT + col] = v;
-                }
-            }
+        }
+        #pragma unroll
+        for (int j8 = 0; j8 < CPT / 8; ++j8) {
+            u16x8 o;
+            #pragma unroll
+            for (int j = 0; j < 8; ++j) o[j] = f2bf(v[8 * j8 + j]);
+            *(u16x8*)&Al[r * 136 + seg * CPT + 8 * j8] = o;
+        }
+    }
+
+    #pragma unroll
+    for (int i = 0; i < 8; ++i) {
+        int chunk = i * 256 + t;
+        int c = chunk >> 4, k8 = chunk & 15;
+        *(u16x8*)&Wl[c * 136 + k8 * 8] = *(const u16x8*)&Wb[(size_t)(co + c) * 128 + k8 * 8];
+    }
+    __syncthreads();
+
+    short8 af[4];
+    #pragma unroll
+    for (int ks = 0; ks < 4; ++ks)
+        af[ks] = *(short8*)&Al[(roww * 16 + la) * 136 + ks * 32 + g * 8];
+    #pragma unroll
+    for (int cti = 0; cti < CT; ++cti) {
+        int ct = colg * CT + cti;
+        f32x4 acc = (f32x4){0.f, 0.f, 0.f, 0.f};
+        #pragma unroll
+        for (int ks = 0; ks < 4; ++ks) {
+            short8 bf = *(short8*)&Wl[(ct * 16 + la) * 136 + ks * 32 + g * 8];
+            acc = __builtin_amdgcn_mfma_f32_16x16x32_bf16(af[ks], bf, acc, 0, 0, 0);
+        }
+        int col = co + ct * 16 + la;
+        float bv = 0.f;
+        if constexpr (BIASF) bv = bias[col];
+        #pragma unroll
+        for (int r = 0; r < 4; ++r) {
+            int row = rb + roww * 16 + g * 4 + r;
+            float v = acc[r] + bv;
+            if constexpr (SCL)  v *= BN_S;
+            if constexpr (ACT)  v = gelu_f(v);
+            if constexpr (QSCL) v *= ATT_SCALE;
+            if constexpr (OUTBF) ((unsigned short*)outv)[(size_t)row * NOT + col] = f2bf(v);
+            else                 ((float*)outv)[(size_t)row * NOT + col] = v;
         }
     }
 }
 
-struct KVJob {
-    const unsigned short* A;
-    const unsigned short* W1;
-    const float* b1;
-    const unsigned short* W2;
-    const float* b2;
-    unsigned short* o1;
-    unsigned short* o2;
-};
-
-__global__ __launch_bounds__(256)
-void k_kvheads(KVJob jk, KVJob jv) {
-    const KVJob j = (blockIdx.x < 288) ? jk : jv;
-    const int rb = (blockIdx.x % 288) * 64;
-    __shared__ unsigned short Al[64 * 136];
-    __shared__ unsigned short Wl[128 * 136];
-    const int t = threadIdx.x;
-    const int lane = t & 63, wv = t >> 6;
-    const int la = lane & 15, g = lane >> 4;
-
-    {
-        int r = t >> 2, seg = t & 3;
-        const unsigned short* ab = j.A + (size_t)(rb + r) * 128 + seg * 32;
-        float v[32];
-        #pragma unroll
-        for (int j8 = 0; j8 < 4; ++j8) {
-            u16x8 raw = *(const u16x8*)&ab[8 * j8];
-            #pragma unroll
-            for (int jj = 0; jj < 8; ++jj) v[8 * j8 + jj] = bf2f(raw[jj]);
-        }
-        float s = 0.f;
-        #pragma unroll
-        for (int jj = 0; jj < 32; ++jj) s += v[jj];
-        s += __shfl_xor(s, 1); s += __shfl_xor(s, 2);
-        float mu = s * (1.0f / 128.0f);
-        float ss = 0.f;
-        #pragma unroll
-        for (int jj = 0; jj < 32; ++jj) { float d = v[jj] - mu; ss += d * d; }
-        ss += __shfl_xor(ss, 1); ss += __shfl_xor(ss, 2);
-        float rs = rsqrtf(ss * (1.0f / 128.0f) + LN_EPS);
-        #pragma unroll
-        for (int j8 = 0; j8 < 4; ++j8) {
-            u16x8 o;
-            #pragma unroll
-            for (int jj = 0; jj < 8; ++jj) o[jj] = f2bf((v[8 * j8 + jj] - mu) * rs);
-            *(u16x8*)&Al[r * 136 + seg * 32 + 8 * j8] = o;
-        }
-    }
-
-    #pragma unroll 1
-    for (int set = 0; set < 2; ++set) {
-        const unsigned short* Wc = set ? j.W2 : j.W1;
-        const float* bc = set ? j.b2 : j.b1;
-        unsigned short* oc = set ? j.o2 : j.o1;
-        if (set) __syncthreads();
-        #pragma unroll
-        for (int i = 0; i < 8; ++i) {
-            int chunk = i * 256 + t;
-            int c = chunk >> 4, k8 = chunk & 15;
-            *(u16x8*)&Wl[c * 136 + k8 * 8] =
-                *(const u16x8*)&Wc[(size_t)c * 128 + k8 * 8];
-        }
-        __syncthreads();
-        short8 af[4];
-        #pragma unroll
-        for (int ks = 0; ks < 4; ++ks)
-            af[ks] = *(short8*)&Al[(wv * 16 + la) * 136 + ks * 32 + g * 8];
-        #pragma unroll
-        for (int ct = 0; ct < 8; ++ct) {
-            f32x4 acc = (f32x4){0.f, 0.f, 0.f, 0.f};
-            #pragma unroll
-            for (int ks = 0; ks < 4; ++ks) {
-                short8 bf = *(short8*)&Wl[(ct * 16 + la) * 136 + ks * 32 + g * 8];
-                acc = __builtin_amdgcn_mfma_f32_16x16x32_bf16(af[ks], bf, acc, 0, 0, 0);
-            }
-            int col = ct * 16 + la;
-            float bv = bc[col];
-            #pragma unroll
-            for (int r = 0; r < 4; ++r) {
-                int row = rb + wv * 16 + g * 4 + r;
-                oc[(size_t)row * 128 + col] = f2bf(acc[r] + bv);
-            }
-        }
-    }
-}
-
-template<int AM>
 __global__ __launch_bounds__(256)
 void k_projmlp(const float* __restrict__ Ain, const unsigned short* __restrict__ pwb,
                const float* __restrict__ pb, const float* __restrict__ resid,
@@ -450,28 +406,10 @@
 
     {
         int r = t >> 4, seg = t & 15;
+        const float* ar = Ain + (size_t)(rb + r) * 128 + seg * 8;
         float v[8];
-        if constexpr (AM == 2) {
-            int hw = rb + r;
-            int h = hw >> 6, w = hw & 63;
-            int l = (h >> 3) * 8 + (w >> 3), ww = (h & 7) * 8 + (w & 7);
-            const float* src = Ain + ((size_t)(l * 64 + ww)) * 6 * 128 + seg * 8;
-            #pragma unroll
-            for (int jj = 0; jj < 8; ++jj) v[jj] = 0.f;
-            #pragma unroll
-            for (int n = 0; n < 6; ++n) {
-                float4 x0 = *(const float4*)&src[n * 128];
-                float4 x1 = *(const float4*)&src[n * 128 + 4];
-                v[0] += x0.x; v[1] += x0.y; v[2] += x0.z; v[3] += x0.w;
-                v[4] += x1.x; v[5] += x1.y; v[6] += x1.z; v[7] += x1.w;
-            }
-            #pragma unroll
-            for (int jj = 0; jj < 8; ++jj) v[jj] *= (1.0f / 6.0f);
-        } else {
-            const float* ar = Ain + (size_t)(rb + r) * 128 + seg * 8;
-            *(float4*)&v[0] = *(const float4*)&ar[0];
-            *(float4*)&v[4] = *(const float4*)&ar[4];
-        }
+        *(float4*)&v[0] = *(const float4*)&ar[0];
+        *(float4*)&v[4] = *(const float4*)&ar[4];
         u16x8 o;
         #pragma unroll
         for (int jj = 0; jj < 8; ++jj) o[jj] = f2bf(v[jj]);
@@ -794,6 +732,11 @@
 
     __shared__ unsigned short Kl[KROWS * 40];
     __shared__ unsigned short Vt[32 * 312];
+    __shared__ float Ol[64 * 33];
+
+    if constexpr (MODE == 1) {
+        for (int i = t; i < 64 * 33; i += T) Ol[i] = 0.f;
+    }
 
     for (int i = t; i < KROWS * 4; i += T) {
         int row = i >> 2, seg = i & 3;
@@ -872,26 +815,44 @@
         }
     }
 
-    #pragma unroll
-    for (int qt = 0; qt < QTPW; ++qt) {
-        float s = srow[qt];
-        s += __shfl_xor(s, 16);
-        s += __shfl_xor(s, 32);
-        #pragma unroll
-        for (int r = 0; r < 4; ++r) {
-            float sq = __shfl(s, g * 4 + r);
-            float inv = 1.0f / sq;
-            int q = (wv * QTPW + qt) * 16 + g * 4 + r;
-            size_t orow;
-            if (MODE == 1) {
-                int n = q >> 6, ww = q & 63;
-                orow = (size_t)(l * 64 + ww) * 6 + n;
-            } else {
-                orow = (size_t)(((q >> 3) * 8 + xw) * 64 + (q & 7) * 8 + yw);
-            }
-            float* ap = aout + orow * 128 + m * DHD;
-            ap[la]      = acc[qt][0][r] * inv;
-            ap[16 + la] = acc[qt][1][r] * inv;
+    if constexpr (MODE == 1) {
+        #pragma unroll
+        for (int qt = 0; qt < QTPW; ++qt) {
+            float s = srow[qt];
+            s += __shfl_xor(s, 16);
+            s += __shfl_xor(s, 32);
+            #pragma unroll
+            for (int r = 0; r < 4; ++r) {
+                float sq = __shfl(s, g * 4 + r);
+                float inv = 1.0f / (6.0f * sq);
+                int q = (wv * QTPW + qt) * 16 + g * 4 + r;
+                int ww = q & 63;
+                atomicAdd(&Ol[ww * 33 + la],      acc[qt][0][r] * inv);
+                atomicAdd(&Ol[ww * 33 + 16 + la], acc[qt][1][r] * inv);
+            }
+        }
+        __syncthreads();
+        for (int i = t; i < 2048; i += T) {
+            int ww = i >> 5, col = i & 31;
+            int h = xw * 8 + (ww >> 3), w = yw * 8 + (ww & 7);
+            aout[(size_t)(h * 64 + w) * 128 + m * 32 + col] = Ol[ww * 33 + col];
+        }
+    } else {
+        #pragma unroll
+        for (int qt = 0; qt < QTPW; ++qt) {
+            float s = srow[qt];
+            s += __shfl_xor(s, 16);
+            s += __shfl_xor(s, 32);
+            #pragma unroll
+            for (int r = 0; r < 4; ++r) {
+                float sq = __shfl(s, g * 4 + r);
+                float inv = 1.0f / sq;
+                int q = (wv * QTPW + qt) * 16 + g * 4 + r;
+                size_t orow = (size_t)(((q >> 3) * 8 + xw) * 64 + (q & 7) * 8 + yw);
+                float* ap = aout + orow * 128 + m * DHD;
+                ap[la]      = acc[qt][0][r] * inv;
+                ap[16 + la] = acc[qt][1][r] * inv;
+            }
         }
     }
 }
@@ -927,16 +888,7 @@
     separt[(size_t)blockIdx.x * 512 + ch] = sacc;
 }
 
-__global__ void k_sered(const float* __restrict__ separt, float* __restrict__ separt2) {
-    int t = threadIdx.x, bb = blockIdx.x;
-    float s = 0.f;
-    #pragma unroll
-    for (int i = 0; i < 16; ++i)
-        s += separt[(size_t)(bb * 16 + i) * 512 + t];
-    separt2[(size_t)bb * 512 + t] = s;
-}
-
-__global__ void k_se(const float* __restrict__ separt2,
+__global__ void k_se(const float* __restrict__ separt,
                      const float* __restrict__ s1w, const float* __restrict__ s1b,
                      const float* __restrict__ s2w, const float* __restrict__ s2b,
                      float* __restrict__ se) {
@@ -944,8 +896,8 @@
     __shared__ float s1[32];
     int t = threadIdx.x;
     float s = 0.f;
-    #pragma unroll
-    for (int b = 0; b < 16; ++b) s += separt2[b * 512 + t];
+    #pragma unroll 8
+    for (int b = 0; b < 256; ++b) s += separt[(size_t)b * 512 + t];
     mean[t] = s * (1.0f / 4096.0f);
     __syncthreads();
     int u = t >> 4, seg = t & 15;
@@ -1019,61 +971,51 @@
     const float* po_b   = (const float*)d_in[48];
 
     float* ws = (float*)d_ws;
-    float* x_cl   = ws + 0;
-    unsigned short* key_b = (unsigned short*)(ws + 524288);
-    unsigned short* val_b = (unsigned short*)(ws + 1703936);
-    unsigned short* qh1b  = (unsigned short*)(ws + 2883584);
-    unsigned short* kh1b  = (unsigned short*)(ws + 4456448);
-    unsigned short* vh1b  = (unsigned short*)(ws + 5636096);
-    unsigned short* kh2b  = (unsigned short*)(ws + 6815744);
-    unsigned short* vh2b  = (unsigned short*)(ws + 7995392);
-    float* abuf   = ws + 9175040;
-    float* qimg   = ws + 12320768;
-    float* qimg2  = ws + 12845056;
-    float* zln    = ws + 13369344;
-    float* abuf2  = ws + 13893632;
-    float* expandb = ws + 14942208;
-    float* dwout   = ws + 17039360;
-    float* separt  = ws + 19136512;
-    float* separt2 = ws + 19267584;
-    float* sebuf   = ws + 19275776;
-    unsigned short* wb = (unsigned short*)(ws + 19276288);
+    float* x_cl = ws + 0;
+    unsigned short* qh1b = (unsigned short*)(ws + 524288);
+    unsigned short* kh1b = (unsigned short*)(ws + 2097152);
+    unsigned short* vh1b = (unsigned short*)(ws + 3276800);
+    unsigned short* kh2b = (unsigned short*)(ws + 4456448);
+    unsigned short* vh2b = (unsigned short*)(ws + 5636096);
+    float* amean  = ws + 6815744;
+    float* qimg   = ws + 7340032;
+    float* qimg2  = ws + 7864320;
+    float* zln    = ws + 8388608;
+    float* abuf2  = ws + 8912896;
+    float* expandb = ws + 9437184;
+    float* dwout   = ws + 11534336;
+    float* separt  = ws + 13631488;
+    float* sebuf   = ws + 13762560;
+    unsigned short* wb = (unsigned short*)(ws + 13763072);
     unsigned short* qh2b = qh1b;
 
-    k_cvtw<<<248, 256, 0, stream>>>(fp_w, fl_w, a1_qw, a1_kw, a2_kw, a1_vw, a2_vw,
+    k_prep<<<760, 256, 0, stream>>>(fp_w, fl_w, a1_qw, a1_kw, a2_kw, a1_vw, a2_vw,
                                     a1_pw, m1_w1, m1_w2, a2_qw, a2_pw, m2_w1, m2_w2,
-                                    mb_ew, mb_pw, pm_w1, pm_w2, po_w, wb);
-    k_transx<<<dim3(128, 4), 256, 0, stream>>>(x, x_cl);
-
-    k_gemm_mfma<64,1,128, 1,0,0,0,0, 0,0,0,1, 1,0,0,1,1><<<288, 256, 0, stream>>>(
-        feat, (const float*)(wb + OFF_FP), ie_w, E_inv, I_inv,
-        (const float*)(wb + OFF_FL), ce_w, val_b, nullptr, key_b);
-
-    k_gemm_mfma<64,1,128, 3,1,1,0,0, 0,0,0,0, 1,1,0,0,1><<<384, 256, 0, stream>>>(
-        nullptr, (const float*)(wb + OFF_A1QW), a1_qb, bev, x_cl, be_w, be_b,
-        (void*)E_inv, (float*)ce_w, qh1b);
-    {
-        KVJob jk = { key_b, wb + OFF_A1KW, a1_kb, wb + OFF_A2KW, a2_kb, kh1b, kh2b };
-        KVJob jv = { val_b, wb + OFF_A1VW, a1_vb, wb + OFF_A2VW, a2_vb, vh1b, vh2b };
-        k_kvheads<<<576, 256, 0, stream>>>(jk, jv);
-    }
-    k_attn_mfma<1><<<dim3(64, HEADS), 512, 0, stream>>>(qh1b, kh1b, vh1b, abuf);
-    k_projmlp<2><<<256, 256, 0, stream>>>(abuf, wb + OFF_A1PW, a1_pb, x_cl,
-                                          wb + OFF_M1W1, m1_b1, wb + OFF_M1W2, m1_b2, qimg);
-
-    k_gemm_mfma<16,1,128, 0,1,1,0,0, 0,0,0,0, 1,1,0,0,1><<<256, 256, 0, stream>>>(
-        qimg, (const float*)(wb + OFF_A2QW), a2_qb, nullptr, nullptr, nullptr,
-        nullptr, nullptr, nullptr, qh2b);
+                                    mb_ew, mb_pw, pm_w1, pm_w2, po_w, wb, x, x_cl);
+
+    k_keyval<<<288, 256, 0, stream>>>(feat, wb, ie_w, ce_w, I_inv, E_inv,
+                                      a1_kb, a2_kb, a1_vb, a2_vb,
+                                      kh1b, kh2b, vh1b, vh2b);
+
+    k_gemm_mfma<64,128,3, 1,1,0,0, 1,1,0><<<384, 256, 0, stream>>>(
+        nullptr, wb + OFF_A1QW, a1_qb, bev, x_cl, be_w, be_b, E_inv, ce_w,
+        nullptr, qh1b);
+    k_attn_mfma<1><<<dim3(64, HEADS), 512, 0, stream>>>(qh1b, kh1b, vh1b, amean);
+    k_projmlp<<<256, 256, 0, stream>>>(amean, wb + OFF_A1PW, a1_pb, x_cl,
+                                       wb + OFF_M1W1, m1_b1, wb + OFF_M1W2, m1_b2, qimg);
+
+    k_gemm_mfma<16,128,0, 1,1,0,0, 1,1,0><<<256, 256, 0, stream>>>(
+        qimg, wb + OFF_A2QW, a2_qb, nullptr, nullptr, nullptr, nullptr, nullptr,
+        nullptr, nullptr, qh2b);
     k_attn_mfma<2><<<dim3(64, HEADS), 256, 0, stream>>>(qh2b, kh2b, vh2b, abuf2);
-    k_projmlp<0><<<256, 256, 0, stream>>>(abuf2, wb + OFF_A2PW, a2_pb, qimg,
-                                          wb + OFF_M2W1, m2_b1, wb + OFF_M2W2, m2_b2, qimg2);
-
-    k_gemm_mfma<16,1,512, 0,1,0,1,1, 0,0,0,0, 0,0,1,0,1><<<dim3(256, 4), 256, 0, stream>>>(
-        qimg2, (const float*)(wb + OFF_MBEW), nullptr, nullptr, nullptr, nullptr,
-        nullptr, nullptr, zln, expandb);
+    k_projmlp<<<256, 256, 0, stream>>>(abuf2, wb + OFF_A2PW, a2_pb, qimg,
+                                       wb + OFF_M2W1, m2_b1, wb + OFF_M2W2, m2_b2, qimg2);
+
+    k_gemm_mfma<16,512,0, 1,0,1,1, 0,0,1><<<dim3(256, 4), 256, 0, stream>>>(
+        qimg2, wb + OFF_MBEW, nullptr, nullptr, nullptr, nullptr, nullptr, nullptr,
+        nullptr, zln, expandb);
     k_dwconv<<<256, 512, 0, stream>>>(expandb, mb_dw, dwout, separt);
-    k_sered<<<16, 512, 0, stream>>>(separt, separt2);
-    k_se<<<1, 512, 0, stream>>>(separt2, mb_s1w, mb_s1b, mb_s2w, mb_s2b, sebuf);
+    k_se<<<1, 512, 0, stream>>>(separt, mb_s1w, mb_s1b, mb_s2w, mb_s2b, sebuf);
     k_mbprojmlp<<<256, 256, 0, stream>>>(dwout, wb + OFF_MBPW, sebuf, zln,
                                          wb + OFF_PMW1, pm_b1, wb + OFF_PMW2, pm_b2,
                                          wb + OFF_POW, po_b, (float*)d_out);
```

After: 172.9 us. +11.4%, slower.
